# Performance work log

Hardware: AMD Instinct MI355X
Metric: run time of the kernel (lower is better)

The kernel has to match this reference:

```python
import jax, jax.numpy as jnp
import numpy as np

C = 8; E = 512; HEADS = 8; DH = E // HEADS; M = 256; PINV_ITERS = 6; KW = 33

def layer_norm(x, g, b):
    mu = x.mean(-1, keepdims=True)
    xm = x - mu
    v = (xm * xm).mean(-1, keepdims=True)
    return xm / jnp.sqrt(v + 1e-5) * g + b

def mp_pinv(x, iters=PINV_ITERS):
    # Moore-Penrose pseudoinverse via Newton-Schulz iterations (lucidrains nystrom-attention)
    I = jnp.eye(x.shape[-1], dtype=x.dtype)
    ax = jnp.abs(x)
    z = jnp.swapaxes(x, -1, -2) / (jnp.max(ax.sum(-2)) * jnp.max(ax.sum(-1)))
    for _ in range(iters):
        xz = x @ z
        z = 0.25 * z @ (13. * I - xz @ (15. * I - xz @ (7. * I - xz)))
    return z

def nystrom_attn(x, mask, Wqkv, Wout, bout, conv_w):
    b, n0, d = x.shape
    pad = (-n0) % M  # left-pad so seq divisible by num_landmarks
    x = jnp.pad(x, ((0, 0), (pad, 0), (0, 0)))
    mask = jnp.pad(mask, ((0, 0), (pad, 0)))
    n = n0 + pad
    qkv = (x @ Wqkv).reshape(b, n, 3, HEADS, DH).transpose(2, 0, 3, 1, 4)
    q, k, v = qkv[0], qkv[1], qkv[2]  # [b,h,n,dh]
    mf = mask[:, None, :, None].astype(x.dtype)
    q = q * mf * (DH ** -0.5); k = k * mf; v = v * mf
    l = n // M
    mls = mask.reshape(b, 1, M, l).sum(-1).astype(x.dtype)  # valid count per landmark segment
    div = mls[..., None] + 1e-8
    ql = q.reshape(b, HEADS, M, l, DH).sum(3) / div
    kl = k.reshape(b, HEADS, M, l, DH).sum(3) / div
    mland = mls > 0  # [b,1,M]
    neg = -jnp.finfo(x.dtype).max / 2
    sim1 = jnp.where(mask[:, None, :, None] & mland[..., None, :], jnp.einsum('bhid,bhjd->bhij', q, kl), neg)
    sim2 = jnp.where(mland[..., :, None] & mland[..., None, :], jnp.einsum('bhid,bhjd->bhij', ql, kl), neg)
    sim3 = jnp.where(mland[..., :, None] & mask[:, None, None, :], jnp.einsum('bhid,bhjd->bhij', ql, k), neg)
    a1 = jax.nn.softmax(sim1, -1); a2 = jax.nn.softmax(sim2, -1); a3 = jax.nn.softmax(sim3, -1)
    out = (a1 @ mp_pinv(a2)) @ (a3 @ v)
    # residual depthwise conv over sequence dim (residual=True in NystromAttention)
    out = out + jax.lax.conv_general_dilated(v, conv_w, (1, 1), ((KW // 2, KW // 2), (0, 0)),
                                             dimension_numbers=('NCHW', 'OIHW', 'NCHW'),
                                             feature_group_count=HEADS)
    out = out.transpose(0, 2, 1, 3).reshape(b, n, d) @ Wout + bout
    return out[:, pad:]

def _forward(h, W1, b1, cls_token, pmt_token, ln1_g, ln1_b, Wqkv1, Wout1, bout1, conv1,
             ln0_g, ln0_b, Wqkv0, Wout0, bout0, conv0, lnf_g, lnf_b, W3, b3):
    N = h.shape[0]
    h1 = jax.nn.relu(h @ W1 + b1)  # _fc1
    seq = jnp.concatenate([cls_token, pmt_token, h1], 0)[None]  # [1, 1+C+N, E]
    y = nystrom_attn(layer_norm(seq, ln1_g, ln1_b), jnp.ones((1, seq.shape[1]), bool),
                     Wqkv1, Wout1, bout1, conv1)
    x = seq + y  # layer1 (TransLayer_custom)
    pmt = x[:, 1:1 + C, :]   # new pmt tokens [1,C,E]
    toks = x[:, 1 + C:, :]   # [1,N,E]
    assn = jax.nn.softmax(jnp.einsum('bnd,bcd->bnc', toks, pmt), -1)
    idx = jnp.argmax(assn[0], -1)  # [N] cluster assignment
    # cluster dispatch: per-cluster [pmt_i; tokens-of-cluster-i] run of shared layer0, via masking
    xs = jnp.concatenate([pmt[0][:, None, :], jnp.broadcast_to(toks[0], (C, N, E))], 1)  # [C,1+N,E]
    masks = jnp.concatenate([jnp.ones((C, 1), bool), idx[None, :] == jnp.arange(C)[:, None]], 1)
    def trans0(xi, mi):
        xi = xi[None]
        return (xi + nystrom_attn(layer_norm(xi, ln0_g, ln0_b), mi[None], Wqkv0, Wout0, bout0, conv0))[0]
    out = jax.vmap(trans0)(xs, masks)  # [C,1+N,E]
    h_un = out[:, 1:, :][idx, jnp.arange(N)]  # each token from its own cluster's run
    order = jnp.argsort(idx)  # stable: groups tokens by cluster, preserving order (concat order)
    h_global = h_un[order]; idx_new = idx[order]
    hcat = jnp.concatenate([x[0, 0][None], h_global], 0)  # [1+N, E]
    hn = layer_norm(hcat, lnf_g, lnf_b)
    sums = jax.ops.segment_sum(hcat[1:], idx_new, num_segments=C)
    counts = jax.ops.segment_sum(jnp.ones((N,), h.dtype), idx_new, num_segments=C)
    merge = sums / jnp.maximum(counts, 1.)[:, None]  # CTM merge token per cluster
    ptc = jnp.linalg.norm(pmt[0] @ pmt[0].T - jnp.eye(C, dtype=h.dtype))
    tok_out = jnp.concatenate([hn[0][None], merge], 0).mean(0)
    logit = tok_out @ W3 + b3
    return logit, ptc

def setup_inputs() -> dict:
    key = jax.random.key(0)
    ks = jax.random.split(key, 16)
    N, IN_DIM, NC = 4096, 1024, 2
    s = 0.02
    q, _ = jnp.linalg.qr(jax.random.normal(ks[15], (E, C)))  # orthonormal pmt init
    return {
        'h': jax.random.normal(ks[0], (N, IN_DIM)),
        'W1': jax.random.normal(ks[1], (IN_DIM, E)) * s, 'b1': jnp.zeros((E,)),
        'cls_token': jax.random.normal(ks[2], (1, E)),
        'pmt_token': q.T,
        'ln1_g': jnp.ones((E,)), 'ln1_b': jnp.zeros((E,)),
        'Wqkv1': jax.random.normal(ks[3], (E, 3 * E)) * s,
        'Wout1': jax.random.normal(ks[4], (E, E)) * s, 'bout1': jnp.zeros((E,)),
        'conv1': jax.random.normal(ks[5], (HEADS, 1, KW, 1)) * s,
        'ln0_g': jnp.ones((E,)), 'ln0_b': jnp.zeros((E,)),
        'Wqkv0': jax.random.normal(ks[6], (E, 3 * E)) * s,
        'Wout0': jax.random.normal(ks[7], (E, E)) * s, 'bout0': jnp.zeros((E,)),
        'conv0': jax.random.normal(ks[8], (HEADS, 1, KW, 1)) * s,
        'lnf_g': jnp.ones((E,)), 'lnf_b': jnp.zeros((E,)),
        'W3': jax.random.normal(ks[9], (E, NC)) * s, 'b3': jnp.zeros((NC,)),
    }

def reference(h, W1, b1, cls_token, pmt_token, ln1_g, ln1_b, Wqkv1, Wout1, bout1, conv1,
              ln0_g, ln0_b, Wqkv0, Wout0, bout0, conv0, lnf_g, lnf_b, W3, b3):
    logit, ptc = _forward(h, W1, b1, cls_token, pmt_token, ln1_g, ln1_b, Wqkv1, Wout1, bout1, conv1,
                          ln0_g, ln0_b, Wqkv0, Wout0, bout0, conv0, lnf_g, lnf_b, W3, b3)
    return (logit[None], jax.nn.softmax(logit)[None], ptc)
```

## Files before the change

### kernel.cpp

```cpp
#include <hip/hip_runtime.h>

#define NEGV (-1.70141173e38f)

constexpr int E    = 512;
constexpr int NTOK = 4096;
constexpr int NPAD = 4352;
constexpr int PAD1 = 247;
constexpr int NSEQ = 4105;
constexpr int NG   = 5120;

typedef __attribute__((ext_vector_type(8))) short short8;
typedef __attribute__((ext_vector_type(4))) float float4v;

__device__ inline float bf2f(ushort u){ return __uint_as_float(((unsigned)u)<<16); }
__device__ inline ushort f2bf(float f){
  unsigned u = __float_as_uint(f);
  unsigned r = (u + 0x7FFFu + ((u>>16)&1u)) >> 16;
  return (ushort)r;
}

template<int BT, bool BOUNDS>
__global__ __launch_bounds__(256) void k_mm(
    const ushort* __restrict__ A, const ushort* __restrict__ B,
    const float* __restrict__ bias, const float* __restrict__ resid,
    float* __restrict__ Cf, ushort* __restrict__ Cb,
    int M, int N, int K, int ksplit, int ldC,
    long sA, long sB, long sC,
    const int* __restrict__ colsel, const int* __restrict__ rowsel,
    int zmodA, int zmodB, const int* __restrict__ krange, int kshift,
    float alpha, float bdiag, int flags)
{
  const int z = blockIdx.z;
  const int batch = z / ksplit, ks = z - batch * ksplit;
  const int kslice = K / ksplit;
  int kbeg = ks * kslice, kend = kbeg + kslice;
  if (krange) { int ki = batch >> kshift; kbeg = krange[2*ki]; kend = krange[2*ki+1]; }
  long aoff;
  if (colsel) { int s = colsel[blockIdx.x]; if (s < 0) s = 0; aoff = (long)(s*8 + batch) * sA; }
  else aoff = (long)(zmodA ? (batch & (zmodA-1)) : batch) * sA;
  long boff;
  if (rowsel) { int s = rowsel[blockIdx.y]; if (s < 0) s = 0; boff = (long)(s*8 + batch) * sB; }
  else boff = (long)(zmodB ? (batch & (zmodB-1)) : batch) * sB;
  A += aoff; B += boff;
  const long coff = (long)z * sC;

  __shared__ __align__(16) ushort Al[4][128][8];
  __shared__ __align__(16) ushort Bl[4][128][8];

  const int tid  = threadIdx.x;
  const int lane = tid & 63, wid = tid >> 6;
  const int wr = wid >> 1, wc = wid & 1;
  const int l4 = lane >> 4, l15 = lane & 15;
  const int row0 = blockIdx.y * 128, col0 = blockIdx.x * 128;

  float4v acc[4][4];
#pragma unroll
  for (int i = 0; i < 4; ++i)
#pragma unroll
    for (int j = 0; j < 4; ++j) acc[i][j] = (float4v){0.f,0.f,0.f,0.f};

  for (int k0 = kbeg; k0 < kend; k0 += 32) {
    __syncthreads();
#pragma unroll
    for (int e = 0; e < 2; ++e) {
      int id = tid * 2 + e; int m = id >> 2, kb = id & 3;
      uint4 v = make_uint4(0u,0u,0u,0u);
      int gr = row0 + m;
      if (!BOUNDS || gr < M)
        v = *reinterpret_cast<const uint4*>(A + (long)gr * K + k0 + kb * 8);
      *reinterpret_cast<uint4*>(&Al[kb][m][0]) = v;
    }
    if (BT) {
#pragma unroll
      for (int e = 0; e < 2; ++e) {
        int id = tid * 2 + e; int n = id >> 2, kb = id & 3;
        uint4 v = make_uint4(0u,0u,0u,0u);
        int gc = col0 + n;
        if (!BOUNDS || gc < N)
          v = *reinterpret_cast<const uint4*>(B + (long)gc * K + k0 + kb * 8);
        *reinterpret_cast<uint4*>(&Bl[kb][n][0]) = v;
      }
    } else {
      int n = tid & 127, gc = col0 + n;
      bool inb = (!BOUNDS || gc < N);
#pragma unroll
      for (int e = 0; e < 2; ++e) {
        int kb = (tid >> 7) * 2 + e;
        ushort u[8];
#pragma unroll
        for (int j = 0; j < 8; ++j) {
          int gk = k0 + kb * 8 + j;
          ushort val = inb ? B[(long)gk * N + gc] : (ushort)0;
          if (flags & 4) {
            float f = bdiag * (gk == gc ? 1.f : 0.f) - bf2f(val);
            val = f2bf(f);
          }
          u[j] = val;
        }
        uint4 w;
        w.x = (unsigned)u[0] | ((unsigned)u[1] << 16);
        w.y = (unsigned)u[2] | ((unsigned)u[3] << 16);
        w.z = (unsigned)u[4] | ((unsigned)u[5] << 16);
        w.w = (unsigned)u[6] | ((unsigned)u[7] << 16);
        *reinterpret_cast<uint4*>(&Bl[kb][n][0]) = w;
      }
    }
    __syncthreads();
    short8 af[4], bg[4];
#pragma unroll
    for (int mi = 0; mi < 4; ++mi)
      af[mi] = *reinterpret_cast<const short8*>(&Al[l4][wr*64 + mi*16 + l15][0]);
#pragma unroll
    for (int ni = 0; ni < 4; ++ni)
      bg[ni] = *reinterpret_cast<const short8*>(&Bl[l4][wc*64 + ni*16 + l15][0]);
#pragma unroll
    for (int mi = 0; mi < 4; ++mi)
#pragma unroll
      for (int ni = 0; ni < 4; ++ni)
        acc[mi][ni] = __builtin_amdgcn_mfma_f32_16x16x32_bf16(af[mi], bg[ni], acc[mi][ni], 0, 0, 0);
  }
#pragma unroll
  for (int mi = 0; mi < 4; ++mi)
#pragma unroll
    for (int ni = 0; ni < 4; ++ni)
#pragma unroll
      for (int r = 0; r < 4; ++r) {
        int row = row0 + wr*64 + mi*16 + l4*4 + r;
        int col = col0 + wc*64 + ni*16 + l15;
        if (BOUNDS && (row >= M || col >= N)) continue;
        float v = alpha * acc[mi][ni][r];
        if (flags & 1) v += bias[col];
        if (flags & 2) v = fmaxf(v, 0.f);
        if (flags & 8) v += resid[(long)row * ldC + col];
        long off = coff + (long)row * ldC + col;
        if (flags & 16) Cb[off] = f2bf(v); else Cf[off] = v;
      }
}

static void mm(hipStream_t st, const void* A, const void* B, const float* bias, const float* resid,
               float* Cf, ushort* Cb, int M, int N, int K, int nb, int ksplit, int ldC,
               long sA, long sB, long sC,
               const int* colsel, const int* rowsel, int zmodA, int zmodB,
               const int* krange, int kshift,
               float alpha, float bdiag, int flags, bool bt, bool bounds)
{
  dim3 g((N + 127) / 128, (M + 127) / 128, nb * ksplit), b(256);
  const ushort* a = (const ushort*)A; const ushort* bb = (const ushort*)B;
  if (bt) {
    if (bounds) k_mm<1, true ><<<g, b, 0, st>>>(a, bb, bias, resid, Cf, Cb, M, N, K, ksplit, ldC, sA, sB, sC, colsel, rowsel, zmodA, zmodB, krange, kshift, alpha, bdiag, flags);
    else        k_mm<1, false><<<g, b, 0, st>>>(a, bb, bias, resid, Cf, Cb, M, N, K, ksplit, ldC, sA, sB, sC, colsel, rowsel, zmodA, zmodB, krange, kshift, alpha, bdiag, flags);
  } else {
    if (bounds) k_mm<0, true ><<<g, b, 0, st>>>(a, bb, bias, resid, Cf, Cb, M, N, K, ksplit, ldC, sA, sB, sC, colsel, rowsel, zmodA, zmodB, krange, kshift, alpha, bdiag, flags);
    else        k_mm<0, false><<<g, b, 0, st>>>(a, bb, bias, resid, Cf, Cb, M, N, K, ksplit, ldC, sA, sB, sC, colsel, rowsel, zmodA, zmodB, krange, kshift, alpha, bdiag, flags);
  }
}

__global__ void k_copy(const float* __restrict__ s, float* __restrict__ d, int n) {
  int i = blockIdx.x * 256 + threadIdx.x;
  if (i < n) d[i] = s[i];
}
__global__ void k_cvt(const float* __restrict__ s, ushort* __restrict__ d, long n) {
  long i = (long)blockIdx.x * 256 + threadIdx.x;
  if (i < n) d[i] = f2bf(s[i]);
}
__global__ void k_tcvt(const float* __restrict__ W, ushort* __restrict__ Wt, int K, int N) {
  __shared__ float tile[32][33];
  int kb = blockIdx.y * 32, nb_ = blockIdx.x * 32;
  int tx = threadIdx.x, ty = threadIdx.y;
  for (int r = ty; r < 32; r += 8) tile[r][tx] = W[(long)(kb + r) * N + nb_ + tx];
  __syncthreads();
  for (int r = ty; r < 32; r += 8) Wt[(long)(nb_ + r) * K + kb + tx] = f2bf(tile[tx][r]);
}

__global__ __launch_bounds__(256) void k_ln(const float* __restrict__ x, const float* __restrict__ g,
                                            const float* __restrict__ b, ushort* __restrict__ y, int rows) {
  int row = blockIdx.x;
  if (row >= rows) return;
  const float* xr = x + (long)row * E;
  __shared__ float red[256];
  int t = threadIdx.x;
  float v0 = xr[t], v1 = xr[t + 256];
  red[t] = v0 + v1; __syncthreads();
  for (int o = 128; o > 0; o >>= 1) { if (t < o) red[t] += red[t + o]; __syncthreads(); }
  float mu = red[0] * (1.f / E); __syncthreads();
  float d0 = v0 - mu, d1 = v1 - mu;
  red[t] = d0 * d0 + d1 * d1; __syncthreads();
  for (int o = 128; o > 0; o >>= 1) { if (t < o) red[t] += red[t + o]; __syncthreads(); }
  float inv = 1.f / sqrtf(red[0] * (1.f / E) + 1e-5f);
  ushort* yr = y + (long)row * E;
  yr[t]       = f2bf(d0 * inv * g[t]       + b[t]);
  yr[t + 256] = f2bf(d1 * inv * g[t + 256] + b[t + 256]);
}

__global__ void k_buildK(const float* __restrict__ qkv, ushort* __restrict__ Kb, int np, int off) {
  long i = (long)blockIdx.x * 256 + threadIdx.x;
  if (i >= (long)np * 512) return;
  int p = (int)(i >> 9), t = (int)(i & 511); int h = t >> 6, d = t & 63;
  Kb[((long)h * np + p) * 64 + d] = f2bf(qkv[(long)p * 1536 + off + t]);
}
__global__ void k_buildVt(const float* __restrict__ qkv, ushort* __restrict__ Vt, int np) {
  int h = blockIdx.y, p0 = blockIdx.x * 64;
  __shared__ float tile[64][65];
  int tx = threadIdx.x & 63, tg = threadIdx.x >> 6;
  for (int r = tg; r < 64; r += 4) tile[r][tx] = qkv[(long)(p0 + r) * 1536 + 1024 + h * 64 + tx];
  __syncthreads();
  for (int d = tg; d < 64; d += 4) Vt[((long)h * 64 + d) * np + p0 + tx] = f2bf(tile[tx][d]);
}

__global__ void k_lm_B(float* __restrict__ divB, float* __restrict__ mlandB) {
  int i = threadIdx.x;
  int cnt = 0;
  for (int j = 0; j < 17; ++j) cnt += (i * 17 + j >= PAD1);
  divB[i] = (float)cnt + 1e-8f;
  mlandB[i] = cnt > 0 ? 1.f : 0.f;
}
__global__ void k_qlkl_B(const float* __restrict__ qkv, const float* __restrict__ divB,
                         ushort* __restrict__ ql, ushort* __restrict__ kl) {
  int i = blockIdx.x, h = blockIdx.y, d = threadIdx.x;
  float sq = 0.f, sk = 0.f;
  for (int j = 0; j < 17; ++j) {
    int p = i * 17 + j;
    if (p >= PAD1) {
      sq += qkv[(long)p * 1536 + h * 64 + d];
      sk += qkv[(long)p * 1536 + 512 + h * 64 + d];
    }
  }
  float dv = divB[i];
  ql[((long)h * 256 + i) * 64 + d] = f2bf(sq * 0.125f / dv);
  kl[((long)h * 256 + i) * 64 + d] = f2bf(sk / dv);
}

__global__ __launch_bounds__(256) void k_a2soft(const float* __restrict__ S2, const float* __restrict__ mland,
                                                ushort* __restrict__ X) {
  int i = blockIdx.x, bt = blockIdx.y, j = threadIdx.x;
  int cl = bt >> 3;
  const float* Sr = S2 + ((long)bt * 256 + i) * 256;
  __shared__ float red[256];
  float landi = mland[cl * 256 + i];
  float out;
  if (landi > 0.f) {
    bool valid = mland[cl * 256 + j] > 0.f;
    float sv = valid ? Sr[j] : NEGV;
    red[j] = sv; __syncthreads();
    for (int o = 128; o > 0; o >>= 1) { if (j < o) red[j] = fmaxf(red[j], red[j + o]); __syncthreads(); }
    float mx = red[0]; __syncthreads();
    float e = valid ? expf(sv - mx) : 0.f;
    red[j] = e; __syncthreads();
    for (int o = 128; o > 0; o >>= 1) { if (j < o) red[j] += red[j + o]; __syncthreads(); }
    out = e / red[0];
  } else {
    out = 1.f / 256.f;
  }
  X[((long)bt * 256 + i) * 256 + j] = f2bf(out);
}

__global__ __launch_bounds__(256) void k_pinv_scale(const ushort* __restrict__ X, float* __restrict__ sc, int nheads) {
  int cl = blockIdx.x, j = threadIdx.x;
  float cmax = -1e30f, rmax = -1e30f;
  for (int h = 0; h < nheads; ++h) {
    const ushort* mat = X + (long)(cl * nheads + h) * 65536;
    float cs = 0.f, rs = 0.f;
    for (int i = 0; i < 256; ++i) { cs += bf2f(mat[i * 256 + j]); rs += bf2f(mat[j * 256 + i]); }
    cmax = fmaxf(cmax, cs); rmax = fmaxf(rmax, rs);
  }
  __shared__ float r1[256], r2[256];
  r1[j] = cmax; r2[j] = rmax; __syncthreads();
  for (int o = 128; o > 0; o >>= 1) {
    if (j < o) { r1[j] = fmaxf(r1[j], r1[j + o]); r2[j] = fmaxf(r2[j], r2[j + o]); }
    __syncthreads();
  }
  if (j == 0) sc[cl] = 1.f / (r1[0] * r2[0]);
}

__global__ void k_z0(const ushort* __restrict__ X, const float* __restrict__ sc, ushort* __restrict__ Z, int nb) {
  long t = (long)blockIdx.x * 256 + threadIdx.x;
  if (t >= (long)nb * 65536) return;
  int bt = (int)(t >> 16); int ij = (int)(t & 65535); int i = ij >> 8, j = ij & 255;
  Z[t] = f2bf(bf2f(X[((long)bt << 16) + j * 256 + i]) * sc[bt >> 3]);
}

__global__ __launch_bounds__(256) void k_smaxB_av(const float* __restrict__ S, ushort* __restrict__ P,
                                                  const float* __restrict__ mland) {
  int i = blockIdx.x, h = blockIdx.y, t = threadIdx.x;
  const float* Sr = S + ((long)h * 256 + i) * NPAD;
  ushort* Pr = P + ((long)h * 256 + i) * NPAD;
  __shared__ float sv[NPAD];
  __shared__ float red[256];
  if (mland[i] > 0.f) {
    float lmax = NEGV;
    for (int j = t; j < NPAD; j += 256) {
      float s = Sr[j];
      sv[j] = s;
      if (j >= PAD1) lmax = fmaxf(lmax, s);
    }
    red[t] = lmax; __syncthreads();
    for (int o = 128; o > 0; o >>= 1) { if (t < o) red[t] = fmaxf(red[t], red[t + o]); __syncthreads(); }
    float mx = red[0]; __syncthreads();
    float lsum = 0.f;
    for (int j = t; j < NPAD; j += 256) {
      float e = (j >= PAD1) ? expf(sv[j] - mx) : 0.f;
      sv[j] = e; lsum += e;
    }
    red[t] = lsum; __syncthreads();
    for (int o = 128; o > 0; o >>= 1) { if (t < o) red[t] += red[t + o]; __syncthreads(); }
    float inv = 1.f / red[0];
    for (int j = t; j < NPAD; j += 256) Pr[j] = f2bf(sv[j] * inv);
  } else {
    const float u = 1.f / 4352.f;
    for (int j = t; j < NPAD; j += 256) Pr[j] = f2bf(j >= PAD1 ? u : 0.f);
  }
}

__global__ __launch_bounds__(256) void k_smaxseg(const float* __restrict__ S3, ushort* __restrict__ P3,
                                                 const float* __restrict__ mlandC, const int* __restrict__ gclu,
                                                 const int* __restrict__ segb) {
  int i = blockIdx.x, bt = blockIdx.y, t = threadIdx.x;
  int c = bt >> 3, h = bt & 7;
  const float* Sr = S3 + ((long)h * 256 + i) * NG;
  ushort* Pr = P3 + ((long)h * 256 + i) * NG;
  int jb = segb[c], je = segb[c + 1];
  __shared__ float sv[4352];
  __shared__ float red[256];
  if (mlandC[c * 256 + i] > 0.f) {
    float lmax = NEGV;
    for (int j = jb + t; j < je; j += 256) {
      float s = Sr[j];
      sv[j - jb] = s;
      if (gclu[j] == c) lmax = fmaxf(lmax, s);
    }
    red[t] = lmax; __syncthreads();
    for (int o = 128; o > 0; o >>= 1) { if (t < o) red[t] = fmaxf(red[t], red[t + o]); __syncthreads(); }
    float mx = red[0]; __syncthreads();
    float lsum = 0.f;
    for (int j = jb + t; j < je; j += 256) {
      float e = (gclu[j] == c) ? expf(sv[j - jb] - mx) : 0.f;
      sv[j - jb] = e; lsum += e;
    }
    red[t] = lsum; __syncthreads();
    for (int o = 128; o > 0; o >>= 1) { if (t < o) red[t] += red[t + o]; __syncthreads(); }
    float inv = 1.f / red[0];
    for (int j = jb + t; j < je; j += 256) Pr[j] = f2bf(sv[j - jb] * inv);
  } else {
    const float u = 1.f / 4352.f;
    for (int j = jb + t; j < je; j += 256) Pr[j] = f2bf(gclu[j] == c ? u : 0.f);
  }
}

template<int MODE>
__global__ __launch_bounds__(256) void k_smax256(const float* __restrict__ S, ushort* __restrict__ P,
                                                 const float* __restrict__ mland, const int* __restrict__ gtok,
                                                 const int* __restrict__ gclu, int rows) {
  int row = blockIdx.x, h = blockIdx.y, j = threadIdx.x;
  const float* Sr = S + ((long)h * rows + row) * 256;
  ushort* Pr = P + ((long)h * rows + row) * 256;
  int c = 0;
  if (MODE == 1) {
    int tk = gtok[row];
    if (tk < 0) { Pr[j] = 0; return; }
    c = gclu[row];
  }
  bool mem = (MODE == 1) ? (mland[c * 256 + j] > 0.f) : (mland[j] > 0.f);
  __shared__ float red[256];
  float s = mem ? Sr[j] : NEGV;
  red[j] = s; __syncthreads();
  for (int o = 128; o > 0; o >>= 1) { if (j < o) red[j] = fmaxf(red[j], red[j + o]); __syncthreads(); }
  float mx = red[0]; __syncthreads();
  float e = mem ? expf(s - mx) : 0.f;
  red[j] = e; __syncthreads();
  for (int o = 128; o > 0; o >>= 1) { if (j < o) red[j] += red[j + o]; __syncthreads(); }
  Pr[j] = f2bf(e / red[0]);
}

__global__ void k_avredB(const float* __restrict__ sl, ushort* __restrict__ avb, int ks) {
  int i = blockIdx.x, h = blockIdx.y, d = threadIdx.x;
  float s = 0.f;
  for (int k = 0; k < ks; ++k) s += sl[(((long)h * ks + k) * 256 + i) * 64 + d];
  avb[((long)h * 256 + i) * 64 + d] = f2bf(s);
}

__global__ void k_conv_B(const float* __restrict__ qkv, const float* __restrict__ w, float* __restrict__ preout) {
  int prow = PAD1 + blockIdx.x, t = threadIdx.x;
  int h = t >> 6;
  float acc = 0.f;
  for (int tt = 0; tt < 33; ++tt) {
    int p = prow + tt - 16;
    if (p >= 0 && p < NPAD) acc += qkv[(long)p * 1536 + 1024 + t] * w[h * 33 + tt];
  }
  preout[(long)prow * E + t] += acc;
}

__global__ void k_idx(const float* __restrict__ x, int* __restrict__ idx) {
  int n = blockIdx.x;
  const float* tok = x + (long)(9 + n) * E;
  const float* pmt = x + E;
  __shared__ float red[64];
  int t = threadIdx.x;
  int c = t >> 3, part = t & 7;
  float s = 0.f;
  for (int d = part * 64; d < part * 64 + 64; ++d) s += tok[d] * pmt[(long)c * E + d];
  red[t] = s; __syncthreads();
  if (t < 8) {
    float dot = 0.f;
    for (int p = 0; p < 8; ++p) dot += red[t * 8 + p];
    red[t] = dot;
  }
  __syncthreads();
  if (t == 0) {
    int best = 0; float bv = red[0];
    for (int c2 = 1; c2 < 8; ++c2) if (red[c2] > bv) { bv = red[c2]; best = c2; }
    idx[n] = best;
  }
}

__global__ void k_ptc(const float* __restrict__ x, float* __restrict__ ptc_out) {
  int t = threadIdx.x;
  int a = t >> 3, b = t & 7;
  const float* pmt = x + E;
  float s = 0.f;
  for (int d = 0; d < E; ++d) s += pmt[(long)a * E + d] * pmt[(long)b * E + d];
  s -= (a == b) ? 1.f : 0.f;
  __shared__ float red[64];
  red[t] = s * s; __syncthreads();
  for (int o = 32; o > 0; o >>= 1) { if (t < o) red[t] += red[t + o]; __syncthreads(); }
  if (t == 0) *ptc_out = sqrtf(red[0]);
}

__global__ void k_lm_C(const int* __restrict__ idx, float* __restrict__ div_c, float* __restrict__ mland_c) {
  int c = blockIdx.x, i = threadIdx.x;
  int cnt = 0;
  for (int j = 0; j < 17; ++j) {
    int p = i * 17 + j;
    if (p == 255) cnt++;
    else if (p >= 256 && idx[p - 256] == c) cnt++;
  }
  div_c[c * 256 + i] = (float)cnt + 1e-8f;
  mland_c[c * 256 + i] = cnt > 0 ? 1.f : 0.f;
}

__global__ void k_qlkl_C(const float* __restrict__ qkv, const float* __restrict__ qkv_pmt,
                         const int* __restrict__ idx, const float* __restrict__ div_c,
                         ushort* __restrict__ qlc, ushort* __restrict__ klc) {
  int i = blockIdx.x, bt = blockIdx.y;
  int c = bt >> 3, h = bt & 7, d = threadIdx.x;
  float sq = 0.f, sk = 0.f;
  for (int j = 0; j < 17; ++j) {
    int p = i * 17 + j;
    const float* src = nullptr;
    if (p == 255) src = qkv_pmt + c * 1536;
    else if (p >= 256 && idx[p - 256] == c) src = qkv + (long)(p - 256) * 1536;
    if (src) { sq += src[h * 64 + d]; sk += src[512 + h * 64 + d]; }
  }
  float dv = div_c[c * 256 + i];
  qlc[((long)bt * 256 + i) * 64 + d] = f2bf(sq * 0.125f / dv);
  klc[((long)bt * 256 + i) * 64 + d] = f2bf(sk / dv);
}

__global__ void k_gcnt(const int* __restrict__ idx, int* __restrict__ scnt) {
  __shared__ int loc[8];
  int b = blockIdx.x, t = threadIdx.x;
  if (t < 8) loc[t] = 0;
  __syncthreads();
  atomicAdd(&loc[idx[b * 256 + t]], 1);
  __syncthreads();
  if (t < 8) scnt[t * 16 + b] = loc[t];
}

__global__ void k_goff(const int* __restrict__ scnt, int* __restrict__ segb, int* __restrict__ boff,
                       int* __restrict__ krange, int* __restrict__ blkclu,
                       int* __restrict__ gtok, int* __restrict__ gclu) {
  if (threadIdx.x != 0) return;
  int s = 0;
  for (int c = 0; c < 8; ++c) {
    segb[c] = s;
    int tot = 1;
    int run = s + 1;
    for (int sl = 0; sl < 16; ++sl) { boff[c * 16 + sl] = run; run += scnt[c * 16 + sl]; tot += scnt[c * 16 + sl]; }
    krange[2 * c] = s;
    krange[2 * c + 1] = s + (((tot + 31) >> 5) << 5);
    gtok[s] = -2 - c; gclu[s] = c;
    s += ((tot + 127) >> 7) << 7;
  }
  segb[8] = s;
  for (int b = 0; b < NG / 128; ++b) {
    int cl = -1;
    for (int c = 0; c < 8; ++c) if (b * 128 >= segb[c] && b * 128 < segb[c + 1]) cl = c;
    blkclu[b] = cl;
  }
}

__global__ void k_gscatter(const int* __restrict__ idx, const int* __restrict__ boff,
                           int* __restrict__ gtok, int* __restrict__ gclu, int* __restrict__ gpos) {
  __shared__ int sidx[256];
  int b = blockIdx.x, t = threadIdx.x;
  int n = b * 256 + t;
  int c = idx[n];
  sidx[t] = c;
  __syncthreads();
  int rank = 0;
  for (int m = 0; m < t; ++m) rank += (sidx[m] == c);
  int pos = boff[c * 16 + b] + rank;
  gtok[pos] = n; gclu[pos] = c; gpos[n] = pos;
}

__global__ void k_gatherQK(const float* __restrict__ qkv, const float* __restrict__ qkv_pmt,
                           const int* __restrict__ gtok, ushort* __restrict__ Qg, ushort* __restrict__ Kg) {
  long i = (long)blockIdx.x * 256 + threadIdx.x;
  if (i >= (long)NG * 512) return;
  int g = (int)(i >> 9), t = (int)(i & 511); int h = t >> 6, d = t & 63;
  int tk = gtok[g];
  float q = 0.f, k = 0.f;
  if (tk >= 0)       { q = qkv[(long)tk * 1536 + t];      k = qkv[(long)tk * 1536 + 512 + t]; }
  else if (tk <= -2) { int c = -2 - tk; q = qkv_pmt[c * 1536 + t]; k = qkv_pmt[c * 1536 + 512 + t]; }
  long o = ((long)h * NG + g) * 64 + d;
  Qg[o] = f2bf(q); Kg[o] = f2bf(k);
}

__global__ void k_gatherVt(const float* __restrict__ qkv, const float* __restrict__ qkv_pmt,
                           const int* __restrict__ gtok, ushort* __restrict__ Vgt) {
  int h = blockIdx.y, p0 = blockIdx.x * 64;
  __shared__ float tile[64][65];
  int tx = threadIdx.x & 63, tg = threadIdx.x >> 6;
  for (int r = tg; r < 64; r += 4) {
    int tk = gtok[p0 + r];
    float v = 0.f;
    if (tk >= 0)       v = qkv[(long)tk * 1536 + 1024 + h * 64 + tx];
    else if (tk <= -2) v = qkv_pmt[(-2 - tk) * 1536 + 1024 + h * 64 + tx];
    tile[r][tx] = v;
  }
  __syncthreads();
  for (int d = tg; d < 64; d += 4) Vgt[((long)h * 64 + d) * NG + p0 + tx] = f2bf(tile[tx][d]);
}

__global__ void k_outC(const float* __restrict__ OUTg, const int* __restrict__ gpos,
                       const int* __restrict__ idx, const float* __restrict__ qkv,
                       const float* __restrict__ qkv_pmt, const float* __restrict__ w,
                       float* __restrict__ OUTA) {
  int n = blockIdx.x, t = threadIdx.x;
  int h = t >> 6;
  int c = idx[n];
  float acc = OUTg[(long)gpos[n] * 512 + t];
  for (int tt = 0; tt < 33; ++tt) {
    int m = n + tt - 16;
    float vv = 0.f;
    if (m == -1) vv = qkv_pmt[c * 1536 + 1024 + t];
    else if (m >= 0 && m < NTOK && idx[m] == c) vv = qkv[(long)m * 1536 + 1024 + t];
    acc += vv * w[h * 33 + tt];
  }
  OUTA[(long)n * E + t] = acc;
}

__global__ void k_seg_part(const float* __restrict__ hun, const int* __restrict__ idx,
                           float* __restrict__ part, float* __restrict__ pcnt) {
  int c = blockIdx.x, sl = blockIdx.y, d = threadIdx.x;
  float s = 0.f; int cnt = 0;
  for (int n = sl * 256; n < sl * 256 + 256; ++n) {
    if (idx[n] == c) { s += hun[(long)n * E + d]; if (d == 0) cnt++; }
  }
  part[(long)(c * 16 + sl) * E + d] = s;
  if (d == 0) pcnt[c * 16 + sl] = (float)cnt;
}

__global__ void k_final(const float* __restrict__ x0, const float* __restrict__ g, const float* __restrict__ b,
                        const float* __restrict__ part, const float* __restrict__ pcnt,
                        const float* __restrict__ ptc, const float* __restrict__ W3, const float* __restrict__ b3,
                        float* __restrict__ out) {
  int t = threadIdx.x;
  __shared__ float red[512];
  float xv = x0[t];
  red[t] = xv; __syncthreads();
  for (int o = 256; o > 0; o >>= 1) { if (t < o) red[t] += red[t + o]; __syncthreads(); }
  float mu = red[0] * (1.f / 512.f); __syncthreads();
  float d0 = xv - mu;
  red[t] = d0 * d0; __syncthreads();
  for (int o = 256; o > 0; o >>= 1) { if (t < o) red[t] += red[t + o]; __syncthreads(); }
  float inv = 1.f / sqrtf(red[0] * (1.f / 512.f) + 1e-5f);
  __syncthreads();
  float acc = d0 * inv * g[t] + b[t];
  for (int c = 0; c < 8; ++c) {
    float s = 0.f, cnt = 0.f;
    for (int sl = 0; sl < 16; ++sl) { s += part[(long)(c * 16 + sl) * E + t]; cnt += pcnt[c * 16 + sl]; }
    acc += s / fmaxf(cnt, 1.f);
  }
  float tk = acc * (1.f / 9.f);
  red[t] = tk * W3[t * 2 + 0]; __syncthreads();
  for (int o = 256; o > 0; o >>= 1) { if (t < o) red[t] += red[t + o]; __syncthreads(); }
  float l0 = red[0] + b3[0]; __syncthreads();
  red[t] = tk * W3[t * 2 + 1]; __syncthreads();
  for (int o = 256; o > 0; o >>= 1) { if (t < o) red[t] += red[t + o]; __syncthreads(); }
  float l1 = red[0] + b3[1];
  if (t == 0) {
    out[0] = l0; out[1] = l1;
    float mx = fmaxf(l0, l1);
    float e0 = expf(l0 - mx), e1 = expf(l1 - mx), s = e0 + e1;
    out[2] = e0 / s; out[3] = e1 / s;
    out[4] = *ptc;
  }
}

static void pinv_iters(hipStream_t st, const ushort* PX, ushort* PZ, ushort* Y, ushort* T1, ushort* T2, int nb) {
  ushort* z = PZ; ushort* y = Y;
  for (int it = 0; it < 6; ++it) {
    mm(st, PX, z,  nullptr, nullptr, nullptr, y,  256,256,256, nb,1,256, 65536,65536,65536, nullptr,nullptr,0,0,nullptr,0, 1.f,   0.f, 16,    false, false);
    mm(st, y,  y,  nullptr, nullptr, nullptr, T1, 256,256,256, nb,1,256, 65536,65536,65536, nullptr,nullptr,0,0,nullptr,0, 1.f,   7.f, 16|4,  false, false);
    mm(st, y,  T1, nullptr, nullptr, nullptr, T2, 256,256,256, nb,1,256, 65536,65536,65536, nullptr,nullptr,0,0,nullptr,0, 1.f,  15.f, 16|4,  false, false);
    mm(st, z,  T2, nullptr, nullptr, nullptr, y,  256,256,256, nb,1,256, 65536,65536,65536, nullptr,nullptr,0,0,nullptr,0, 0.25f,13.f, 16|4,  false, false);
    ushort* tmp = z; z = y; y = tmp;
  }
}

extern "C" void kernel_launch(void* const* d_in, const int* in_sizes, int n_in,
                              void* d_out, int out_size, void* d_ws, size_t ws_size,
                              hipStream_t stream) {
  const float* h_in  = (const float*)d_in[0];
  const float* W1    = (const float*)d_in[1];
  const float* b1    = (const float*)d_in[2];
  const float* cls   = (const float*)d_in[3];
  const float* pmt_t = (const float*)d_in[4];
  const float* ln1_g = (const float*)d_in[5];
  const float* ln1_b = (const float*)d_in[6];
  const float* Wqkv1 = (const float*)d_in[7];
  const float* Wout1 = (const float*)d_in[8];
  const float* bout1 = (const float*)d_in[9];
  const float* conv1 = (const float*)d_in[10];
  const float* ln0_g = (const float*)d_in[11];
  const float* ln0_b = (const float*)d_in[12];
  const float* Wqkv0 = (const float*)d_in[13];
  const float* Wout0 = (const float*)d_in[14];
  const float* bout0 = (const float*)d_in[15];
  const float* conv0 = (const float*)d_in[16];
  const float* lnf_g = (const float*)d_in[17];
  const float* lnf_b = (const float*)d_in[18];
  const float* W3    = (const float*)d_in[19];
  const float* b3    = (const float*)d_in[20];

  char* base = (char*)d_ws;
  size_t off = 0;
  auto alloc = [&](size_t b) -> void* {
    off = (off + 255) & ~(size_t)255;
    void* p = base + off; off += b; return p;
  };
  float*  SEQ    = (float*) alloc((size_t)NSEQ * E * 4);
  float*  QKV    = (float*) alloc((size_t)NPAD * 1536 * 4);
  float*  QKVPMT = (float*) alloc(8 * 1536 * 4);
  ushort* W1t    = (ushort*)alloc((size_t)512 * 1024 * 2);
  ushort* Wq1t   = (ushort*)alloc((size_t)1536 * 512 * 2);
  ushort* Wq0t   = (ushort*)alloc((size_t)1536 * 512 * 2);
  ushort* Wo1t   = (ushort*)alloc((size_t)512 * 512 * 2);
  ushort* Wo0t   = (ushort*)alloc((size_t)512 * 512 * 2);
  ushort* LNb    = (ushort*)alloc((size_t)NPAD * E * 2);
  ushort* LNPMTb = (ushort*)alloc(8 * 512 * 2);
  ushort* QbU    = (ushort*)alloc((size_t)8 * NG * 64 * 2);
  ushort* KbU    = (ushort*)alloc((size_t)8 * NG * 64 * 2);
  ushort* VtU    = (ushort*)alloc((size_t)8 * NG * 64 * 2);
  char*   U1     = (char*)  alloc((size_t)8 * 256 * NG * 4);
  char*   U2     = (char*)  alloc((size_t)8 * 256 * NG * 2);
  ushort* PXb    = (ushort*)alloc((size_t)64 * 65536 * 2);
  ushort* PZa    = (ushort*)alloc((size_t)64 * 65536 * 2);
  ushort* qlbB   = (ushort*)alloc((size_t)8 * 16384 * 2);
  ushort* klbB   = (ushort*)alloc((size_t)8 * 16384 * 2);
  ushort* qlcb   = (ushort*)alloc((size_t)64 * 16384 * 2);
  ushort* klcb   = (ushort*)alloc((size_t)64 * 16384 * 2);
  float*  avsl   = (float*) alloc((size_t)8 * 8 * 16384 * 4);
  ushort* avb    = (ushort*)alloc((size_t)64 * 16384 * 2);
  ushort* Wcb    = (ushort*)alloc((size_t)64 * 16384 * 2);
  float*  PREOUT = (float*) alloc((size_t)NPAD * E * 4);
  float*  OUTA   = (float*) alloc((size_t)NTOK * E * 4);
  float*  divB   = (float*) alloc(256 * 4);
  float*  mlandB = (float*) alloc(256 * 4);
  float*  divC   = (float*) alloc(8 * 256 * 4);
  float*  mlandC = (float*) alloc(8 * 256 * 4);
  int*    idx    = (int*)   alloc(NTOK * 4);
  int*    gtok   = (int*)   alloc(NG * 4);
  int*    gclu   = (int*)   alloc(NG * 4);
  int*    gpos   = (int*)   alloc(NTOK * 4);
  int*    scnt   = (int*)   alloc(8 * 16 * 4);
  int*    boffA  = (int*)   alloc(8 * 16 * 4);
  int*    segb   = (int*)   alloc(9 * 4);
  int*    krange = (int*)   alloc(16 * 4);
  int*    blkclu = (int*)   alloc((NG / 128) * 4);
  float*  ptc    = (float*) alloc(256);
  float*  sc     = (float*) alloc(256);
  float*  part   = (float*) alloc((size_t)8 * 16 * 512 * 4);
  float*  pcnt   = (float*) alloc(8 * 16 * 4);

  ushort* hb   = (ushort*)U1;
  float*  Sbuf = (float*)U1;
  ushort* Ybuf = (ushort*)U1;
  ushort* T1   = (ushort*)(U1 + (size_t)64 * 65536 * 2);
  ushort* T2   = (ushort*)(U1 + (size_t)2 * 64 * 65536 * 2);
  float*  OUTg = (float*)U1;
  ushort* Pbuf = (ushort*)U2;

  k_tcvt<<<dim3(512/32, 1024/32), dim3(32,8), 0, stream>>>(W1, W1t, 1024, 512);
  k_tcvt<<<dim3(1536/32, 512/32), dim3(32,8), 0, stream>>>(Wqkv1, Wq1t, 512, 1536);
  k_tcvt<<<dim3(1536/32, 512/32), dim3(32,8), 0, stream>>>(Wqkv0, Wq0t, 512, 1536);
  k_tcvt<<<dim3(512/32, 512/32),  dim3(32,8), 0, stream>>>(Wout1, Wo1t, 512, 512);
  k_tcvt<<<dim3(512/32, 512/32),  dim3(32,8), 0, stream>>>(Wout0, Wo0t, 512, 512);

  k_copy<<<dim3(2),  dim3(256), 0, stream>>>(cls,   SEQ,       512);
  k_copy<<<dim3(16), dim3(256), 0, stream>>>(pmt_t, SEQ + 512, 4096);
  k_cvt<<<dim3(16384), dim3(256), 0, stream>>>(h_in, hb, (long)4096 * 1024);
  mm(stream, hb, W1t, b1, nullptr, SEQ + 9 * 512, nullptr, 4096, 512, 1024, 1, 1, 512,
     0, 0, 0, nullptr, nullptr, 0, 0, nullptr, 0, 1.f, 0.f, 1 | 2, true, false);

  hipMemsetAsync(LNb, 0, (size_t)PAD1 * E * 2, stream);
  k_ln<<<dim3(NSEQ), dim3(256), 0, stream>>>(SEQ, ln1_g, ln1_b, LNb + (long)PAD1 * E, NSEQ);
  mm(stream, LNb, Wq1t, nullptr, nullptr, QKV, nullptr, NPAD, 1536, 512, 1, 1, 1536,
     0, 0, 0, nullptr, nullptr, 0, 0, nullptr, 0, 1.f, 0.f, 0, true, false);
  k_buildK<<<dim3((NPAD*512)/256), dim3(256), 0, stream>>>(QKV, QbU, NPAD, 0);
  k_buildK<<<dim3((NPAD*512)/256), dim3(256), 0, stream>>>(QKV, KbU, NPAD, 512);
  k_buildVt<<<dim3(NPAD/64, 8), dim3(256), 0, stream>>>(QKV, VtU, NPAD);
  k_lm_B<<<dim3(1), dim3(256), 0, stream>>>(divB, mlandB);
  k_qlkl_B<<<dim3(256, 8), dim3(64), 0, stream>>>(QKV, divB, qlbB, klbB);
  mm(stream, qlbB, klbB, nullptr, nullptr, Sbuf, nullptr, 256, 256, 64, 8, 1, 256,
     16384, 16384, 65536, nullptr, nullptr, 0, 0, nullptr, 0, 1.f, 0.f, 0, true, false);
  k_a2soft<<<dim3(256, 8), dim3(256), 0, stream>>>(Sbuf, mlandB, PXb);
  k_pinv_scale<<<dim3(1), dim3(256), 0, stream>>>(PXb, sc, 8);
  k_z0<<<dim3((8*65536)/256), dim3(256), 0, stream>>>(PXb, sc, PZa, 8);
  pinv_iters(stream, PXb, PZa, Ybuf, T1, T2, 8);
  mm(stream, qlbB, KbU, nullptr, nullptr, Sbuf, nullptr, 256, NPAD, 64, 8, 1, NPAD,
     16384, (long)NPAD*64, (long)256*NPAD, nullptr, nullptr, 0, 0, nullptr, 0, 1.f, 0.f, 0, true, false);
  k_smaxB_av<<<dim3(256, 8), dim3(256), 0, stream>>>(Sbuf, Pbuf, mlandB);
  mm(stream, Pbuf, VtU, nullptr, nullptr, avsl, nullptr, 256, 64, NPAD, 8, 8, 64,
     (long)256*NPAD, (long)64*NPAD, 16384, nullptr, nullptr, 0, 0, nullptr, 0, 1.f, 0.f, 0, true, true);
  k_avredB<<<dim3(256, 8), dim3(64), 0, stream>>>(avsl, avb, 8);
  mm(stream, PZa, avb, nullptr, nullptr, nullptr, Wcb, 256, 64, 256, 8, 1, 64,
     65536, 16384, 16384, nullptr, nullptr, 0, 0, nullptr, 0, 1.f, 0.f, 16, false, true);
  mm(stream, QbU + PAD1*64, klbB, nullptr, nullptr, Sbuf, nullptr, NSEQ, 256, 64, 8, 1, 256,
     (long)NPAD*64, 16384, (long)NSEQ*256, nullptr, nullptr, 0, 0, nullptr, 0, 0.125f, 0.f, 0, true, true);
  k_smax256<0><<<dim3(NSEQ, 8), dim3(256), 0, stream>>>(Sbuf, Pbuf, mlandB, nullptr, nullptr, NSEQ);
  mm(stream, Pbuf, Wcb, nullptr, nullptr, PREOUT + (long)PAD1*512, nullptr, NSEQ, 64, 256, 8, 1, 512,
     (long)NSEQ*256, 16384, 64, nullptr, nullptr, 0, 0, nullptr, 0, 1.f, 0.f, 0, false, true);
  k_conv_B<<<dim3(NSEQ), dim3(512), 0, stream>>>(QKV, conv1, PREOUT);
  k_cvt<<<dim3((NSEQ*512 + 255)/256), dim3(256), 0, stream>>>(PREOUT + (long)PAD1*E, LNb, (long)NSEQ * 512);
  mm(stream, LNb, Wo1t, bout1, SEQ, SEQ, nullptr, NSEQ, 512, 512, 1, 1, 512,
     0, 0, 0, nullptr, nullptr, 0, 0, nullptr, 0, 1.f, 0.f, 1 | 8, true, true);

  k_idx<<<dim3(NTOK), dim3(64), 0, stream>>>(SEQ, idx);
  k_ptc<<<dim3(1), dim3(64), 0, stream>>>(SEQ, ptc);
  hipMemsetAsync(gtok, 0xFF, NG * 4, stream);
  hipMemsetAsync(gclu, 0xFF, NG * 4, stream);
  k_gcnt<<<dim3(16), dim3(256), 0, stream>>>(idx, scnt);
  k_goff<<<dim3(1), dim3(64), 0, stream>>>(scnt, segb, boffA, krange, blkclu, gtok, gclu);
  k_gscatter<<<dim3(16), dim3(256), 0, stream>>>(idx, boffA, gtok, gclu, gpos);
  k_ln<<<dim3(NTOK), dim3(256), 0, stream>>>(SEQ + 9 * 512, ln0_g, ln0_b, LNb, NTOK);
  k_ln<<<dim3(8), dim3(256), 0, stream>>>(SEQ + 512, ln0_g, ln0_b, LNPMTb, 8);
  mm(stream, LNb, Wq0t, nullptr, nullptr, QKV, nullptr, NTOK, 1536, 512, 1, 1, 1536,
     0, 0, 0, nullptr, nullptr, 0, 0, nullptr, 0, 1.f, 0.f, 0, true, false);
  mm(stream, LNPMTb, Wq0t, nullptr, nullptr, QKVPMT, nullptr, 8, 1536, 512, 1, 1, 1536,
     0, 0, 0, nullptr, nullptr, 0, 0, nullptr, 0, 1.f, 0.f, 0, true, true);
  k_lm_C<<<dim3(8), dim3(256), 0, stream>>>(idx, divC, mlandC);
  k_qlkl_C<<<dim3(256, 64), dim3(64), 0, stream>>>(QKV, QKVPMT, idx, divC, qlcb, klcb);
  k_gatherQK<<<dim3((NG*512)/256), dim3(256), 0, stream>>>(QKV, QKVPMT, gtok, QbU, KbU);
  k_gatherVt<<<dim3(NG/64, 8), dim3(256), 0, stream>>>(QKV, QKVPMT, gtok, VtU);
  mm(stream, qlcb, klcb, nullptr, nullptr, Sbuf, nullptr, 256, 256, 64, 64, 1, 256,
     16384, 16384, 65536, nullptr, nullptr, 0, 0, nullptr, 0, 1.f, 0.f, 0, true, false);
  k_a2soft<<<dim3(256, 64), dim3(256), 0, stream>>>(Sbuf, mlandC, PXb);
  k_pinv_scale<<<dim3(8), dim3(256), 0, stream>>>(PXb, sc, 8);
  k_z0<<<dim3((64*65536)/256), dim3(256), 0, stream>>>(PXb, sc, PZa, 64);
  pinv_iters(stream, PXb, PZa, Ybuf, T1, T2, 64);
  mm(stream, qlcb, KbU, nullptr, nullptr, Sbuf, nullptr, 256, NG, 64, 8, 1, NG,
     16384, (long)NG*64, (long)256*NG, blkclu, nullptr, 0, 0, nullptr, 0, 1.f, 0.f, 0, true, false);
  k_smaxseg<<<dim3(256, 64), dim3(256), 0, stream>>>(Sbuf, Pbuf, mlandC, gclu, segb);
  mm(stream, Pbuf, VtU, nullptr, nullptr, nullptr, avb, 256, 64, NG, 64, 1, 64,
     (long)256*NG, (long)64*NG, 16384, nullptr, nullptr, 8, 8, krange, 3, 1.f, 0.f, 16, true, true);
  mm(stream, PZa, avb, nullptr, nullptr, nullptr, Wcb, 256, 64, 256, 64, 1, 64,
     65536, 16384, 16384, nullptr, nullptr, 0, 0, nullptr, 0, 1.f, 0.f, 16, false, true);
  mm(stream, QbU, klcb, nullptr, nullptr, Sbuf, nullptr, NG, 256, 64, 8, 1, 256,
     (long)NG*64, 16384, (long)NG*256, nullptr, blkclu, 0, 0, nullptr, 0, 0.125f, 0.f, 0, true, false);
  k_smax256<1><<<dim3(NG, 8), dim3(256), 0, stream>>>(Sbuf, Pbuf, mlandC, gtok, gclu, NG);
  mm(stream, Pbuf, Wcb, nullptr, nullptr, OUTg, nullptr, NG, 64, 256, 8, 1, 512,
     (long)NG*256, 16384, 64, nullptr, blkclu, 0, 0, nullptr, 0, 1.f, 0.f, 0, false, true);
  k_outC<<<dim3(NTOK), dim3(512), 0, stream>>>(OUTg, gpos, idx, QKV, QKVPMT, conv0, OUTA);
  k_cvt<<<dim3((NTOK*512)/256), dim3(256), 0, stream>>>(OUTA, LNb, (long)NTOK * 512);
  mm(stream, LNb, Wo0t, bout0, SEQ + 9 * 512, PREOUT, nullptr, NTOK, 512, 512, 1, 1, 512,
     0, 0, 0, nullptr, nullptr, 0, 0, nullptr, 0, 1.f, 0.f, 1 | 8, true, false);

  k_seg_part<<<dim3(8, 16), dim3(512), 0, stream>>>(PREOUT, idx, part, pcnt);
  k_final<<<dim3(1), dim3(512), 0, stream>>>(SEQ, lnf_g, lnf_b, part, pcnt, ptc, W3, b3,
                                             (float*)d_out);
}
```

Baseline: 2.712 ms.

## Fuse pinv Newton-Schulz loop into one kernel and merge many small kernels

```diff
diff --git a/kernel.cpp b/kernel.cpp
--- a/kernel.cpp
+++ b/kernel.cpp
@@ -8,6 +8,7 @@
 constexpr int PAD1 = 247;
 constexpr int NSEQ = 4105;
 constexpr int NG   = 5120;
+constexpr int NTP  = 4104;
 
 typedef __attribute__((ext_vector_type(8))) short short8;
 typedef __attribute__((ext_vector_type(4))) float float4v;
@@ -17,6 +18,14 @@
   unsigned u = __float_as_uint(f);
   unsigned r = (u + 0x7FFFu + ((u>>16)&1u)) >> 16;
   return (ushort)r;
+}
+__device__ inline short8 pack8u(const ushort* u) {
+  union { short8 v; unsigned w[4]; } x;
+  x.w[0] = (unsigned)u[0] | ((unsigned)u[1] << 16);
+  x.w[1] = (unsigned)u[2] | ((unsigned)u[3] << 16);
+  x.w[2] = (unsigned)u[4] | ((unsigned)u[5] << 16);
+  x.w[3] = (unsigned)u[6] | ((unsigned)u[7] << 16);
+  return x.v;
 }
 
 template<int BT, bool BOUNDS>
@@ -155,30 +164,227 @@
   }
 }
 
-__global__ void k_copy(const float* __restrict__ s, float* __restrict__ d, int n) {
+__device__ __forceinline__ void gsync() {
+  __threadfence();
+  __syncthreads();
+}
+
+template<int AMODE, int BMODE>
+__device__ __forceinline__ void wg_gemm256(
+    const ushort* __restrict__ Ag, const ushort* __restrict__ Bg,
+    ushort (* __restrict__ Yl)[256], ushort (* __restrict__ Btl)[256],
+    float4v acc[8][4], int tid)
+{
+  const int lane = tid & 63;
+  const int wid  = tid >> 6;
+  const int wr = wid >> 2, wc = wid & 3;
+  const int l4 = lane >> 4, l15 = lane & 15;
+#pragma unroll 1
+  for (int kt = 0; kt < 8; ++kt) {
+    const int k0 = kt * 32;
+    if (BMODE == 0) {
+      __syncthreads();
+      int kk = tid >> 4, n0 = (tid & 15) * 16;
+      int s = (kk >> 3) << 4;
+      const ushort* src = Bg + (long)(k0 + kk) * 256 + n0;
+      *reinterpret_cast<uint4*>(&Btl[kk][n0 ^ s])       = *reinterpret_cast<const uint4*>(src);
+      *reinterpret_cast<uint4*>(&Btl[kk][(n0 + 8) ^ s]) = *reinterpret_cast<const uint4*>(src + 8);
+      __syncthreads();
+    }
+    short8 af[8];
+#pragma unroll
+    for (int mi = 0; mi < 8; ++mi) {
+      int r = wr * 128 + mi * 16 + l15;
+      if (AMODE == 0) {
+        af[mi] = *reinterpret_cast<const short8*>(Ag + (long)r * 256 + k0 + l4 * 8);
+      } else {
+        int sr = ((r >> 3) & 3) << 4;
+        af[mi] = *reinterpret_cast<const short8*>(&Yl[r][(k0 + l4 * 8) ^ sr]);
+      }
+    }
+    short8 bf[4];
+#pragma unroll
+    for (int ni = 0; ni < 4; ++ni) {
+      int c = wc * 64 + ni * 16 + l15;
+      ushort u[8];
+      if (BMODE == 0) {
+        int kb = l4 * 8;
+        int cc = c ^ ((kb >> 3) << 4);
+#pragma unroll
+        for (int j = 0; j < 8; ++j) u[j] = Btl[kb + j][cc];
+      } else {
+        int kb = k0 + l4 * 8;
+        int cc = c ^ (((kb >> 3) & 3) << 4);
+#pragma unroll
+        for (int j = 0; j < 8; ++j) u[j] = Yl[kb + j][cc];
+      }
+      bf[ni] = pack8u(u);
+    }
+#pragma unroll
+    for (int mi = 0; mi < 8; ++mi)
+#pragma unroll
+      for (int ni = 0; ni < 4; ++ni)
+        acc[mi][ni] = __builtin_amdgcn_mfma_f32_16x16x32_bf16(af[mi], bf[ni], acc[mi][ni], 0, 0, 0);
+  }
+}
+
+__global__ __launch_bounds__(512) void k_pinv_chain(
+    const ushort* __restrict__ Xall, ushort* __restrict__ ZAall, ushort* __restrict__ ZBall,
+    ushort* __restrict__ T1all, ushort* __restrict__ T2all, const float* __restrict__ sc)
+{
+  __shared__ ushort Yl[256][256];
+  __shared__ ushort Btl[32][256];
+  const int bt = blockIdx.x;
+  const ushort* X = Xall + (long)bt * 65536;
+  ushort* Z0 = ZAall + (long)bt * 65536;
+  ushort* Z1 = ZBall + (long)bt * 65536;
+  ushort* T1 = T1all + (long)bt * 65536;
+  ushort* T2 = T2all + (long)bt * 65536;
+  const int tid = threadIdx.x;
+  const int lane = tid & 63, wid = tid >> 6;
+  const int wr = wid >> 2, wc = wid & 3;
+  const int l4 = lane >> 4, l15 = lane & 15;
+  const float scale = sc[bt >> 3];
+
+  {
+    int r = tid & 255, half = tid >> 8;
+    for (int c0 = half * 128; c0 < half * 128 + 128; c0 += 8) {
+      ushort u[8];
+#pragma unroll
+      for (int j = 0; j < 8; ++j)
+        u[j] = f2bf(bf2f(X[(long)(c0 + j) * 256 + r]) * scale);
+      *reinterpret_cast<short8*>(Z0 + (long)r * 256 + c0) = pack8u(u);
+    }
+  }
+  gsync();
+
+  ushort* Zc = Z0;
+  ushort* Zn = Z1;
+  float4v acc[8][4];
+
+  for (int it = 0; it < 6; ++it) {
+#pragma unroll
+    for (int i = 0; i < 8; ++i)
+#pragma unroll
+      for (int j = 0; j < 4; ++j) acc[i][j] = (float4v){0.f,0.f,0.f,0.f};
+    wg_gemm256<0,0>(X, Zc, Yl, Btl, acc, tid);
+    __syncthreads();
+#pragma unroll
+    for (int mi = 0; mi < 8; ++mi)
+#pragma unroll
+      for (int ni = 0; ni < 4; ++ni)
+#pragma unroll
+        for (int ri = 0; ri < 4; ++ri) {
+          int row = wr*128 + mi*16 + l4*4 + ri;
+          int col = wc*64 + ni*16 + l15;
+          Yl[row][col ^ (((row >> 3) & 3) << 4)] = f2bf(acc[mi][ni][ri]);
+        }
+    __syncthreads();
+#pragma unroll
+    for (int i = 0; i < 8; ++i)
+#pragma unroll
+      for (int j = 0; j < 4; ++j) acc[i][j] = (float4v){0.f,0.f,0.f,0.f};
+    wg_gemm256<1,1>(nullptr, nullptr, Yl, Btl, acc, tid);
+#pragma unroll
+    for (int mi = 0; mi < 8; ++mi)
+#pragma unroll
+      for (int ni = 0; ni < 4; ++ni)
+#pragma unroll
+        for (int ri = 0; ri < 4; ++ri) {
+          int row = wr*128 + mi*16 + l4*4 + ri;
+          int col = wc*64 + ni*16 + l15;
+          float y = bf2f(Yl[row][col ^ (((row >> 3) & 3) << 4)]);
+          T1[(long)row*256 + col] = f2bf(7.f*y - acc[mi][ni][ri]);
+        }
+    gsync();
+#pragma unroll
+    for (int i = 0; i < 8; ++i)
+#pragma unroll
+      for (int j = 0; j < 4; ++j) acc[i][j] = (float4v){0.f,0.f,0.f,0.f};
+    wg_gemm256<1,0>(nullptr, T1, Yl, Btl, acc, tid);
+#pragma unroll
+    for (int mi = 0; mi < 8; ++mi)
+#pragma unroll
+      for (int ni = 0; ni < 4; ++ni)
+#pragma unroll
+        for (int ri = 0; ri < 4; ++ri) {
+          int row = wr*128 + mi*16 + l4*4 + ri;
+          int col = wc*64 + ni*16 + l15;
+          float y = bf2f(Yl[row][col ^ (((row >> 3) & 3) << 4)]);
+          T2[(long)row*256 + col] = f2bf(15.f*y - acc[mi][ni][ri]);
+        }
+    gsync();
+#pragma unroll
+    for (int i = 0; i < 8; ++i)
+#pragma unroll
+      for (int j = 0; j < 4; ++j) acc[i][j] = (float4v){0.f,0.f,0.f,0.f};
+    wg_gemm256<0,0>(Zc, T2, Yl, Btl, acc, tid);
+#pragma unroll
+    for (int mi = 0; mi < 8; ++mi)
+#pragma unroll
+      for (int ni = 0; ni < 4; ++ni)
+#pragma unroll
+        for (int ri = 0; ri < 4; ++ri) {
+          int row = wr*128 + mi*16 + l4*4 + ri;
+          int col = wc*64 + ni*16 + l15;
+          float zv = bf2f(Zc[(long)row*256 + col]);
+          Zn[(long)row*256 + col] = f2bf(0.25f*(13.f*zv - acc[mi][ni][ri]));
+        }
+    gsync();
+    ushort* tmp = Zc; Zc = Zn; Zn = tmp;
+  }
+}
+
+__global__ __launch_bounds__(256) void k_colmax(const ushort* __restrict__ X, float* __restrict__ sc) {
+  int cl = blockIdx.x, j = threadIdx.x;
+  float cmax = 0.f;
+  for (int h = 0; h < 8; ++h) {
+    const ushort* mat = X + (long)(cl * 8 + h) * 65536;
+    float cs = 0.f;
+    for (int i = 0; i < 256; ++i) cs += bf2f(mat[i * 256 + j]);
+    cmax = fmaxf(cmax, cs);
+  }
+  __shared__ float red[256];
+  red[j] = cmax; __syncthreads();
+  for (int o = 128; o > 0; o >>= 1) { if (j < o) red[j] = fmaxf(red[j], red[j + o]); __syncthreads(); }
+  if (j == 0) sc[cl] = 1.f / red[0];
+}
+
+__global__ void k_prep0(const float* __restrict__ cls, const float* __restrict__ pmt, float* __restrict__ seq) {
   int i = blockIdx.x * 256 + threadIdx.x;
-  if (i < n) d[i] = s[i];
+  if (i < 512) seq[i] = cls[i];
+  else if (i < 4608) seq[i] = pmt[i - 512];
 }
 __global__ void k_cvt(const float* __restrict__ s, ushort* __restrict__ d, long n) {
   long i = (long)blockIdx.x * 256 + threadIdx.x;
   if (i < n) d[i] = f2bf(s[i]);
 }
-__global__ void k_tcvt(const float* __restrict__ W, ushort* __restrict__ Wt, int K, int N) {
+__global__ void k_tcvt_all(const float* __restrict__ W1, const float* __restrict__ Wq1,
+                           const float* __restrict__ Wq0, const float* __restrict__ Wo1,
+                           const float* __restrict__ Wo0,
+                           ushort* __restrict__ W1t, ushort* __restrict__ Wq1t,
+                           ushort* __restrict__ Wq0t, ushort* __restrict__ Wo1t,
+                           ushort* __restrict__ Wo0t) {
+  const float* W; ushort* Wt; int K, N;
+  switch (blockIdx.z) {
+    case 0:  W = W1;  Wt = W1t;  K = 1024; N = 512;  break;
+    case 1:  W = Wq1; Wt = Wq1t; K = 512;  N = 1536; break;
+    case 2:  W = Wq0; Wt = Wq0t; K = 512;  N = 1536; break;
+    case 3:  W = Wo1; Wt = Wo1t; K = 512;  N = 512;  break;
+    default: W = Wo0; Wt = Wo0t; K = 512;  N = 512;  break;
+  }
+  int nb_ = blockIdx.x * 32, kb = blockIdx.y * 32;
+  if (nb_ >= N || kb >= K) return;
   __shared__ float tile[32][33];
-  int kb = blockIdx.y * 32, nb_ = blockIdx.x * 32;
   int tx = threadIdx.x, ty = threadIdx.y;
   for (int r = ty; r < 32; r += 8) tile[r][tx] = W[(long)(kb + r) * N + nb_ + tx];
   __syncthreads();
   for (int r = ty; r < 32; r += 8) Wt[(long)(nb_ + r) * K + kb + tx] = f2bf(tile[tx][r]);
 }
 
-__global__ __launch_bounds__(256) void k_ln(const float* __restrict__ x, const float* __restrict__ g,
-                                            const float* __restrict__ b, ushort* __restrict__ y, int rows) {
-  int row = blockIdx.x;
-  if (row >= rows) return;
-  const float* xr = x + (long)row * E;
-  __shared__ float red[256];
-  int t = threadIdx.x;
+__device__ __forceinline__ void ln_row(const float* __restrict__ xr, const float* __restrict__ g,
+                                       const float* __restrict__ b, ushort* __restrict__ yr,
+                                       float* red, int t) {
   float v0 = xr[t], v1 = xr[t + 256];
   red[t] = v0 + v1; __syncthreads();
   for (int o = 128; o > 0; o >>= 1) { if (t < o) red[t] += red[t + o]; __syncthreads(); }
@@ -187,47 +393,101 @@
   red[t] = d0 * d0 + d1 * d1; __syncthreads();
   for (int o = 128; o > 0; o >>= 1) { if (t < o) red[t] += red[t + o]; __syncthreads(); }
   float inv = 1.f / sqrtf(red[0] * (1.f / E) + 1e-5f);
-  ushort* yr = y + (long)row * E;
   yr[t]       = f2bf(d0 * inv * g[t]       + b[t]);
   yr[t + 256] = f2bf(d1 * inv * g[t + 256] + b[t + 256]);
 }
 
-__global__ void k_buildK(const float* __restrict__ qkv, ushort* __restrict__ Kb, int np, int off) {
-  long i = (long)blockIdx.x * 256 + threadIdx.x;
-  if (i >= (long)np * 512) return;
-  int p = (int)(i >> 9), t = (int)(i & 511); int h = t >> 6, d = t & 63;
-  Kb[((long)h * np + p) * 64 + d] = f2bf(qkv[(long)p * 1536 + off + t]);
-}
-__global__ void k_buildVt(const float* __restrict__ qkv, ushort* __restrict__ Vt, int np) {
+__global__ __launch_bounds__(256) void k_lnB(const float* __restrict__ x, const float* __restrict__ g,
+                                             const float* __restrict__ b, ushort* __restrict__ y) {
+  int row = blockIdx.x, t = threadIdx.x;
+  ushort* yr = y + (long)row * E;
+  if (row < PAD1) { yr[t] = 0; yr[t + 256] = 0; return; }
+  __shared__ float red[256];
+  ln_row(x + (long)(row - PAD1) * E, g, b, yr, red, t);
+}
+__global__ __launch_bounds__(256) void k_lnC(const float* __restrict__ seq, const float* __restrict__ g,
+                                             const float* __restrict__ b, ushort* __restrict__ y) {
+  int row = blockIdx.x, t = threadIdx.x;
+  const float* xr = (row < 8) ? (seq + 512 + (long)row * E) : (seq + 9 * 512 + (long)(row - 8) * E);
+  __shared__ float red[256];
+  ln_row(xr, g, b, y + (long)row * E, red, t);
+}
+
+__global__ void k_buildQKVB(const float* __restrict__ qkv, ushort* __restrict__ Qb,
+                            ushort* __restrict__ Kb, ushort* __restrict__ Vt) {
   int h = blockIdx.y, p0 = blockIdx.x * 64;
+  int tx = threadIdx.x & 63, tg = threadIdx.x >> 6;
   __shared__ float tile[64][65];
+  for (int r = tg; r < 64; r += 4) {
+    long src = (long)(p0 + r) * 1536 + h * 64 + tx;
+    long o = ((long)h * NPAD + p0 + r) * 64 + tx;
+    Qb[o] = f2bf(qkv[src]);
+    Kb[o] = f2bf(qkv[src + 512]);
+    tile[r][tx] = qkv[src + 1024];
+  }
+  __syncthreads();
+  for (int d = tg; d < 64; d += 4) Vt[((long)h * 64 + d) * NPAD + p0 + tx] = f2bf(tile[tx][d]);
+}
+__global__ void k_gatherQKV(const float* __restrict__ qkvall, const int* __restrict__ gtok,
+                            ushort* __restrict__ Qg, ushort* __restrict__ Kg, ushort* __restrict__ Vgt) {
+  int h = blockIdx.y, p0 = blockIdx.x * 64;
   int tx = threadIdx.x & 63, tg = threadIdx.x >> 6;
-  for (int r = tg; r < 64; r += 4) tile[r][tx] = qkv[(long)(p0 + r) * 1536 + 1024 + h * 64 + tx];
+  __shared__ float tile[64][65];
+  for (int r = tg; r < 64; r += 4) {
+    int tk = gtok[p0 + r];
+    int srcrow = tk >= 0 ? 8 + tk : (tk <= -2 ? (-2 - tk) : -1);
+    float q = 0.f, k = 0.f, v = 0.f;
+    if (srcrow >= 0) {
+      long s = (long)srcrow * 1536 + h * 64 + tx;
+      q = qkvall[s]; k = qkvall[s + 512]; v = qkvall[s + 1024];
+    }
+    long o = ((long)h * NG + p0 + r) * 64 + tx;
+    Qg[o] = f2bf(q); Kg[o] = f2bf(k);
+    tile[r][tx] = v;
+  }
   __syncthreads();
-  for (int d = tg; d < 64; d += 4) Vt[((long)h * 64 + d) * np + p0 + tx] = f2bf(tile[tx][d]);
-}
-
-__global__ void k_lm_B(float* __restrict__ divB, float* __restrict__ mlandB) {
-  int i = threadIdx.x;
-  int cnt = 0;
-  for (int j = 0; j < 17; ++j) cnt += (i * 17 + j >= PAD1);
-  divB[i] = (float)cnt + 1e-8f;
-  mlandB[i] = cnt > 0 ? 1.f : 0.f;
-}
-__global__ void k_qlkl_B(const float* __restrict__ qkv, const float* __restrict__ divB,
-                         ushort* __restrict__ ql, ushort* __restrict__ kl) {
+  for (int d = tg; d < 64; d += 4) Vgt[((long)h * 64 + d) * NG + p0 + tx] = f2bf(tile[tx][d]);
+}
+
+__global__ void k_qlkl_B(const float* __restrict__ qkv, ushort* __restrict__ ql, ushort* __restrict__ kl,
+                         float* __restrict__ mlandB) {
   int i = blockIdx.x, h = blockIdx.y, d = threadIdx.x;
-  float sq = 0.f, sk = 0.f;
+  float sq = 0.f, sk = 0.f; int cnt = 0;
   for (int j = 0; j < 17; ++j) {
     int p = i * 17 + j;
     if (p >= PAD1) {
       sq += qkv[(long)p * 1536 + h * 64 + d];
       sk += qkv[(long)p * 1536 + 512 + h * 64 + d];
-    }
-  }
-  float dv = divB[i];
+      cnt++;
+    }
+  }
+  float dv = (float)cnt + 1e-8f;
   ql[((long)h * 256 + i) * 64 + d] = f2bf(sq * 0.125f / dv);
   kl[((long)h * 256 + i) * 64 + d] = f2bf(sk / dv);
+  if (h == 0 && d == 0) mlandB[i] = cnt > 0 ? 1.f : 0.f;
+}
+
+__global__ void k_qlkl_C(const float* __restrict__ qkvall, const int* __restrict__ idx,
+                         ushort* __restrict__ qlc, ushort* __restrict__ klc,
+                         float* __restrict__ mland_c) {
+  int i = blockIdx.x, bt = blockIdx.y;
+  int c = bt >> 3, h = bt & 7, d = threadIdx.x;
+  float sq = 0.f, sk = 0.f; int cnt = 0;
+  for (int j = 0; j < 17; ++j) {
+    int p = i * 17 + j;
+    int srcrow = -1;
+    if (p == 255) srcrow = c;
+    else if (p >= 256 && idx[p - 256] == c) srcrow = 8 + (p - 256);
+    if (srcrow >= 0) {
+      const float* src = qkvall + (long)srcrow * 1536 + h * 64;
+      sq += src[d]; sk += src[512 + d];
+      cnt++;
+    }
+  }
+  float dv = (float)cnt + 1e-8f;
+  qlc[((long)bt * 256 + i) * 64 + d] = f2bf(sq * 0.125f / dv);
+  klc[((long)bt * 256 + i) * 64 + d] = f2bf(sk / dv);
+  if (h == 0 && d == 0) mland_c[c * 256 + i] = cnt > 0 ? 1.f : 0.f;
 }
 
 __global__ __launch_bounds__(256) void k_a2soft(const float* __restrict__ S2, const float* __restrict__ mland,
@@ -254,31 +514,6 @@
   X[((long)bt * 256 + i) * 256 + j] = f2bf(out);
 }
 
-__global__ __launch_bounds__(256) void k_pinv_scale(const ushort* __restrict__ X, float* __restrict__ sc, int nheads) {
-  int cl = blockIdx.x, j = threadIdx.x;
-  float cmax = -1e30f, rmax = -1e30f;
-  for (int h = 0; h < nheads; ++h) {
-    const ushort* mat = X + (long)(cl * nheads + h) * 65536;
-    float cs = 0.f, rs = 0.f;
-    for (int i = 0; i < 256; ++i) { cs += bf2f(mat[i * 256 + j]); rs += bf2f(mat[j * 256 + i]); }
-    cmax = fmaxf(cmax, cs); rmax = fmaxf(rmax, rs);
-  }
-  __shared__ float r1[256], r2[256];
-  r1[j] = cmax; r2[j] = rmax; __syncthreads();
-  for (int o = 128; o > 0; o >>= 1) {
-    if (j < o) { r1[j] = fmaxf(r1[j], r1[j + o]); r2[j] = fmaxf(r2[j], r2[j + o]); }
-    __syncthreads();
-  }
-  if (j == 0) sc[cl] = 1.f / (r1[0] * r2[0]);
-}
-
-__global__ void k_z0(const ushort* __restrict__ X, const float* __restrict__ sc, ushort* __restrict__ Z, int nb) {
-  long t = (long)blockIdx.x * 256 + threadIdx.x;
-  if (t >= (long)nb * 65536) return;
-  int bt = (int)(t >> 16); int ij = (int)(t & 65535); int i = ij >> 8, j = ij & 255;
-  Z[t] = f2bf(bf2f(X[((long)bt << 16) + j * 256 + i]) * sc[bt >> 3]);
-}
-
 __global__ __launch_bounds__(256) void k_smaxB_av(const float* __restrict__ S, ushort* __restrict__ P,
                                                   const float* __restrict__ mland) {
   int i = blockIdx.x, h = blockIdx.y, t = threadIdx.x;
@@ -378,23 +613,36 @@
   avb[((long)h * 256 + i) * 64 + d] = f2bf(s);
 }
 
-__global__ void k_conv_B(const float* __restrict__ qkv, const float* __restrict__ w, float* __restrict__ preout) {
-  int prow = PAD1 + blockIdx.x, t = threadIdx.x;
+__global__ void k_conv_B(const float* __restrict__ qkv, const float* __restrict__ w,
+                         const float* __restrict__ preout, ushort* __restrict__ lnb) {
+  int r = blockIdx.x, t = threadIdx.x;
   int h = t >> 6;
-  float acc = 0.f;
+  int prow = PAD1 + r;
+  float acc = preout[(long)prow * E + t];
   for (int tt = 0; tt < 33; ++tt) {
     int p = prow + tt - 16;
-    if (p >= 0 && p < NPAD) acc += qkv[(long)p * 1536 + 1024 + t] * w[h * 33 + tt];
-  }
-  preout[(long)prow * E + t] += acc;
-}
-
-__global__ void k_idx(const float* __restrict__ x, int* __restrict__ idx) {
+    if (p < NPAD) acc += qkv[(long)p * 1536 + 1024 + t] * w[h * 33 + tt];
+  }
+  lnb[(long)r * E + t] = f2bf(acc);
+}
+
+__global__ void k_idxptc(const float* __restrict__ x, int* __restrict__ idx, float* __restrict__ ptc_out) {
+  int t = threadIdx.x;
+  __shared__ float red[64];
+  if (blockIdx.x == NTOK) {
+    int a = t >> 3, b = t & 7;
+    const float* pmt = x + E;
+    float s = 0.f;
+    for (int d = 0; d < E; ++d) s += pmt[(long)a * E + d] * pmt[(long)b * E + d];
+    s -= (a == b) ? 1.f : 0.f;
+    red[t] = s * s; __syncthreads();
+    for (int o = 32; o > 0; o >>= 1) { if (t < o) red[t] += red[t + o]; __syncthreads(); }
+    if (t == 0) *ptc_out = sqrtf(red[0]);
+    return;
+  }
   int n = blockIdx.x;
   const float* tok = x + (long)(9 + n) * E;
   const float* pmt = x + E;
-  __shared__ float red[64];
-  int t = threadIdx.x;
   int c = t >> 3, part = t & 7;
   float s = 0.f;
   for (int d = part * 64; d < part * 64 + 64; ++d) s += tok[d] * pmt[(long)c * E + d];
@@ -412,129 +660,57 @@
   }
 }
 
-__global__ void k_ptc(const float* __restrict__ x, float* __restrict__ ptc_out) {
+__global__ __launch_bounds__(256) void k_gprep(const int* __restrict__ idx, int* __restrict__ gtok,
+                                               int* __restrict__ gclu, int* __restrict__ gpos,
+                                               int* __restrict__ segb, int* __restrict__ krange,
+                                               int* __restrict__ blkclu) {
+  __shared__ int hist[8][16];
+  __shared__ int boff[8][16];
+  __shared__ int segs[9];
+  __shared__ int sidx[256];
   int t = threadIdx.x;
-  int a = t >> 3, b = t & 7;
-  const float* pmt = x + E;
-  float s = 0.f;
-  for (int d = 0; d < E; ++d) s += pmt[(long)a * E + d] * pmt[(long)b * E + d];
-  s -= (a == b) ? 1.f : 0.f;
-  __shared__ float red[64];
-  red[t] = s * s; __syncthreads();
-  for (int o = 32; o > 0; o >>= 1) { if (t < o) red[t] += red[t + o]; __syncthreads(); }
-  if (t == 0) *ptc_out = sqrtf(red[0]);
-}
-
-__global__ void k_lm_C(const int* __restrict__ idx, float* __restrict__ div_c, float* __restrict__ mland_c) {
-  int c = blockIdx.x, i = threadIdx.x;
-  int cnt = 0;
-  for (int j = 0; j < 17; ++j) {
-    int p = i * 17 + j;
-    if (p == 255) cnt++;
-    else if (p >= 256 && idx[p - 256] == c) cnt++;
-  }
-  div_c[c * 256 + i] = (float)cnt + 1e-8f;
-  mland_c[c * 256 + i] = cnt > 0 ? 1.f : 0.f;
-}
-
-__global__ void k_qlkl_C(const float* __restrict__ qkv, const float* __restrict__ qkv_pmt,
-                         const int* __restrict__ idx, const float* __restrict__ div_c,
-                         ushort* __restrict__ qlc, ushort* __restrict__ klc) {
-  int i = blockIdx.x, bt = blockIdx.y;
-  int c = bt >> 3, h = bt & 7, d = threadIdx.x;
-  float sq = 0.f, sk = 0.f;
-  for (int j = 0; j < 17; ++j) {
-    int p = i * 17 + j;
-    const float* src = nullptr;
-    if (p == 255) src = qkv_pmt + c * 1536;
-    else if (p >= 256 && idx[p - 256] == c) src = qkv + (long)(p - 256) * 1536;
-    if (src) { sq += src[h * 64 + d]; sk += src[512 + h * 64 + d]; }
-  }
-  float dv = div_c[c * 256 + i];
-  qlc[((long)bt * 256 + i) * 64 + d] = f2bf(sq * 0.125f / dv);
-  klc[((long)bt * 256 + i) * 64 + d] = f2bf(sk / dv);
-}
-
-__global__ void k_gcnt(const int* __restrict__ idx, int* __restrict__ scnt) {
-  __shared__ int loc[8];
-  int b = blockIdx.x, t = threadIdx.x;
-  if (t < 8) loc[t] = 0;
+  if (t < 128) ((int*)hist)[t] = 0;
   __syncthreads();
-  atomicAdd(&loc[idx[b * 256 + t]], 1);
+  for (int b = 0; b < 16; ++b) atomicAdd(&hist[idx[b * 256 + t]][b], 1);
   __syncthreads();
-  if (t < 8) scnt[t * 16 + b] = loc[t];
-}
-
-__global__ void k_goff(const int* __restrict__ scnt, int* __restrict__ segb, int* __restrict__ boff,
-                       int* __restrict__ krange, int* __restrict__ blkclu,
-                       int* __restrict__ gtok, int* __restrict__ gclu) {
-  if (threadIdx.x != 0) return;
-  int s = 0;
-  for (int c = 0; c < 8; ++c) {
-    segb[c] = s;
-    int tot = 1;
-    int run = s + 1;
-    for (int sl = 0; sl < 16; ++sl) { boff[c * 16 + sl] = run; run += scnt[c * 16 + sl]; tot += scnt[c * 16 + sl]; }
-    krange[2 * c] = s;
-    krange[2 * c + 1] = s + (((tot + 31) >> 5) << 5);
-    gtok[s] = -2 - c; gclu[s] = c;
-    s += ((tot + 127) >> 7) << 7;
-  }
-  segb[8] = s;
-  for (int b = 0; b < NG / 128; ++b) {
+  if (t == 0) {
+    int s = 0;
+    for (int c = 0; c < 8; ++c) {
+      segs[c] = s;
+      int run = s + 1, tot = 1;
+      for (int b = 0; b < 16; ++b) { boff[c][b] = run; run += hist[c][b]; tot += hist[c][b]; }
+      krange[2 * c] = s;
+      krange[2 * c + 1] = s + ((tot + 31) & ~31);
+      s += (tot + 127) & ~127;
+    }
+    segs[8] = s;
+    for (int c = 0; c <= 8; ++c) segb[c] = segs[c];
+  }
+  __syncthreads();
+  for (int g = t; g < NG; g += 256) { gtok[g] = -1; gclu[g] = -1; }
+  __syncthreads();
+  if (t < 8) { gtok[segs[t]] = -2 - t; gclu[segs[t]] = t; }
+  for (int b = t; b < NG / 128; b += 256) {
     int cl = -1;
-    for (int c = 0; c < 8; ++c) if (b * 128 >= segb[c] && b * 128 < segb[c + 1]) cl = c;
+    for (int c = 0; c < 8; ++c) if (b * 128 >= segs[c] && b * 128 < segs[c + 1]) cl = c;
     blkclu[b] = cl;
   }
-}
-
-__global__ void k_gscatter(const int* __restrict__ idx, const int* __restrict__ boff,
-                           int* __restrict__ gtok, int* __restrict__ gclu, int* __restrict__ gpos) {
-  __shared__ int sidx[256];
-  int b = blockIdx.x, t = threadIdx.x;
-  int n = b * 256 + t;
-  int c = idx[n];
-  sidx[t] = c;
-  __syncthreads();
-  int rank = 0;
-  for (int m = 0; m < t; ++m) rank += (sidx[m] == c);
-  int pos = boff[c * 16 + b] + rank;
-  gtok[pos] = n; gclu[pos] = c; gpos[n] = pos;
-}
-
-__global__ void k_gatherQK(const float* __restrict__ qkv, const float* __restrict__ qkv_pmt,
-                           const int* __restrict__ gtok, ushort* __restrict__ Qg, ushort* __restrict__ Kg) {
-  long i = (long)blockIdx.x * 256 + threadIdx.x;
-  if (i >= (long)NG * 512) return;
-  int g = (int)(i >> 9), t = (int)(i & 511); int h = t >> 6, d = t & 63;
-  int tk = gtok[g];
-  float q = 0.f, k = 0.f;
-  if (tk >= 0)       { q = qkv[(long)tk * 1536 + t];      k = qkv[(long)tk * 1536 + 512 + t]; }
-  else if (tk <= -2) { int c = -2 - tk; q = qkv_pmt[c * 1536 + t]; k = qkv_pmt[c * 1536 + 512 + t]; }
-  long o = ((long)h * NG + g) * 64 + d;
-  Qg[o] = f2bf(q); Kg[o] = f2bf(k);
-}
-
-__global__ void k_gatherVt(const float* __restrict__ qkv, const float* __restrict__ qkv_pmt,
-                           const int* __restrict__ gtok, ushort* __restrict__ Vgt) {
-  int h = blockIdx.y, p0 = blockIdx.x * 64;
-  __shared__ float tile[64][65];
-  int tx = threadIdx.x & 63, tg = threadIdx.x >> 6;
-  for (int r = tg; r < 64; r += 4) {
-    int tk = gtok[p0 + r];
-    float v = 0.f;
-    if (tk >= 0)       v = qkv[(long)tk * 1536 + 1024 + h * 64 + tx];
-    else if (tk <= -2) v = qkv_pmt[(-2 - tk) * 1536 + 1024 + h * 64 + tx];
-    tile[r][tx] = v;
-  }
-  __syncthreads();
-  for (int d = tg; d < 64; d += 4) Vgt[((long)h * 64 + d) * NG + p0 + tx] = f2bf(tile[tx][d]);
+  for (int b = 0; b < 16; ++b) {
+    int n = b * 256 + t;
+    int c = idx[n];
+    sidx[t] = c;
+    __syncthreads();
+    int rank = 0;
+    for (int m = 0; m < t; ++m) rank += (sidx[m] == c);
+    int pos = boff[c][b] + rank;
+    gtok[pos] = n; gclu[pos] = c; gpos[n] = pos;
+    __syncthreads();
+  }
 }
 
 __global__ void k_outC(const float* __restrict__ OUTg, const int* __restrict__ gpos,
-                       const int* __restrict__ idx, const float* __restrict__ qkv,
-                       const float* __restrict__ qkv_pmt, const float* __restrict__ w,
-                       float* __restrict__ OUTA) {
+                       const int* __restrict__ idx, const float* __restrict__ qkvall,
+                       const float* __restrict__ w, ushort* __restrict__ lnb) {
   int n = blockIdx.x, t = threadIdx.x;
   int h = t >> 6;
   int c = idx[n];
@@ -542,11 +718,11 @@
   for (int tt = 0; tt < 33; ++tt) {
     int m = n + tt - 16;
     float vv = 0.f;
-    if (m == -1) vv = qkv_pmt[c * 1536 + 1024 + t];
-    else if (m >= 0 && m < NTOK && idx[m] == c) vv = qkv[(long)m * 1536 + 1024 + t];
+    if (m == -1) vv = qkvall[(long)c * 1536 + 1024 + t];
+    else if (m >= 0 && m < NTOK && idx[m] == c) vv = qkvall[(long)(8 + m) * 1536 + 1024 + t];
     acc += vv * w[h * 33 + tt];
   }
-  OUTA[(long)n * E + t] = acc;
+  lnb[(long)n * E + t] = f2bf(acc);
 }
 
 __global__ void k_seg_part(const float* __restrict__ hun, const int* __restrict__ idx,
@@ -594,17 +770,6 @@
     float e0 = expf(l0 - mx), e1 = expf(l1 - mx), s = e0 + e1;
     out[2] = e0 / s; out[3] = e1 / s;
     out[4] = *ptc;
-  }
-}
-
-static void pinv_iters(hipStream_t st, const ushort* PX, ushort* PZ, ushort* Y, ushort* T1, ushort* T2, int nb) {
-  ushort* z = PZ; ushort* y = Y;
-  for (int it = 0; it < 6; ++it) {
-    mm(st, PX, z,  nullptr, nullptr, nullptr, y,  256,256,256, nb,1,256, 65536,65536,65536, nullptr,nullptr,0,0,nullptr,0, 1.f,   0.f, 16,    false, false);
-    mm(st, y,  y,  nullptr, nullptr, nullptr, T1, 256,256,256, nb,1,256, 65536,65536,65536, nullptr,nullptr,0,0,nullptr,0, 1.f,   7.f, 16|4,  false, false);
-    mm(st, y,  T1, nullptr, nullptr, nullptr, T2, 256,256,256, nb,1,256, 65536,65536,65536, nullptr,nullptr,0,0,nullptr,0, 1.f,  15.f, 16|4,  false, false);
-    mm(st, z,  T2, nullptr, nullptr, nullptr, y,  256,256,256, nb,1,256, 65536,65536,65536, nullptr,nullptr,0,0,nullptr,0, 0.25f,13.f, 16|4,  false, false);
-    ushort* tmp = z; z = y; y = tmp;
   }
 }
 
@@ -641,14 +806,12 @@
   };
   float*  SEQ    = (float*) alloc((size_t)NSEQ * E * 4);
   float*  QKV    = (float*) alloc((size_t)NPAD * 1536 * 4);
-  float*  QKVPMT = (float*) alloc(8 * 1536 * 4);
   ushort* W1t    = (ushort*)alloc((size_t)512 * 1024 * 2);
   ushort* Wq1t   = (ushort*)alloc((size_t)1536 * 512 * 2);
   ushort* Wq0t   = (ushort*)alloc((size_t)1536 * 512 * 2);
   ushort* Wo1t   = (ushort*)alloc((size_t)512 * 512 * 2);
   ushort* Wo0t   = (ushort*)alloc((size_t)512 * 512 * 2);
   ushort* LNb    = (ushort*)alloc((size_t)NPAD * E * 2);
-  ushort* LNPMTb = (ushort*)alloc(8 * 512 * 2);
   ushort* QbU    = (ushort*)alloc((size_t)8 * NG * 64 * 2);
   ushort* KbU    = (ushort*)alloc((size_t)8 * NG * 64 * 2);
   ushort* VtU    = (ushort*)alloc((size_t)8 * NG * 64 * 2);
@@ -664,17 +827,12 @@
   ushort* avb    = (ushort*)alloc((size_t)64 * 16384 * 2);
   ushort* Wcb    = (ushort*)alloc((size_t)64 * 16384 * 2);
   float*  PREOUT = (float*) alloc((size_t)NPAD * E * 4);
-  float*  OUTA   = (float*) alloc((size_t)NTOK * E * 4);
-  float*  divB   = (float*) alloc(256 * 4);
   float*  mlandB = (float*) alloc(256 * 4);
-  float*  divC   = (float*) alloc(8 * 256 * 4);
   float*  mlandC = (float*) alloc(8 * 256 * 4);
   int*    idx    = (int*)   alloc(NTOK * 4);
   int*    gtok   = (int*)   alloc(NG * 4);
   int*    gclu   = (int*)   alloc(NG * 4);
   int*    gpos   = (int*)   alloc(NTOK * 4);
-  int*    scnt   = (int*)   alloc(8 * 16 * 4);
-  int*    boffA  = (int*)   alloc(8 * 16 * 4);
   int*    segb   = (int*)   alloc(9 * 4);
   int*    krange = (int*)   alloc(16 * 4);
   int*    blkclu = (int*)   alloc((NG / 128) * 4);
@@ -685,94 +843,71 @@
 
   ushort* hb   = (ushort*)U1;
   float*  Sbuf = (float*)U1;
-  ushort* Ybuf = (ushort*)U1;
-  ushort* T1   = (ushort*)(U1 + (size_t)64 * 65536 * 2);
-  ushort* T2   = (ushort*)(U1 + (size_t)2 * 64 * 65536 * 2);
+  ushort* ZBc  = (ushort*)U1;
+  ushort* T1c  = (ushort*)(U1 + (size_t)64 * 65536 * 2);
+  ushort* T2c  = (ushort*)(U1 + (size_t)2 * 64 * 65536 * 2);
   float*  OUTg = (float*)U1;
   ushort* Pbuf = (ushort*)U2;
 
-  k_tcvt<<<dim3(512/32, 1024/32), dim3(32,8), 0, stream>>>(W1, W1t, 1024, 512);
-  k_tcvt<<<dim3(1536/32, 512/32), dim3(32,8), 0, stream>>>(Wqkv1, Wq1t, 512, 1536);
-  k_tcvt<<<dim3(1536/32, 512/32), dim3(32,8), 0, stream>>>(Wqkv0, Wq0t, 512, 1536);
-  k_tcvt<<<dim3(512/32, 512/32),  dim3(32,8), 0, stream>>>(Wout1, Wo1t, 512, 512);
-  k_tcvt<<<dim3(512/32, 512/32),  dim3(32,8), 0, stream>>>(Wout0, Wo0t, 512, 512);
-
-  k_copy<<<dim3(2),  dim3(256), 0, stream>>>(cls,   SEQ,       512);
-  k_copy<<<dim3(16), dim3(256), 0, stream>>>(pmt_t, SEQ + 512, 4096);
+  k_tcvt_all<<<dim3(48, 32, 5), dim3(32, 8), 0, stream>>>(W1, Wqkv1, Wqkv0, Wout1, Wout0,
+                                                          W1t, Wq1t, Wq0t, Wo1t, Wo0t);
+  k_prep0<<<dim3(18), dim3(256), 0, stream>>>(cls, pmt_t, SEQ);
   k_cvt<<<dim3(16384), dim3(256), 0, stream>>>(h_in, hb, (long)4096 * 1024);
   mm(stream, hb, W1t, b1, nullptr, SEQ + 9 * 512, nullptr, 4096, 512, 1024, 1, 1, 512,
      0, 0, 0, nullptr, nullptr, 0, 0, nullptr, 0, 1.f, 0.f, 1 | 2, true, false);
 
-  hipMemsetAsync(LNb, 0, (size_t)PAD1 * E * 2, stream);
-  k_ln<<<dim3(NSEQ), dim3(256), 0, stream>>>(SEQ, ln1_g, ln1_b, LNb + (long)PAD1 * E, NSEQ);
+  k_lnB<<<dim3(NPAD), dim3(256), 0, stream>>>(SEQ, ln1_g, ln1_b, LNb);
   mm(stream, LNb, Wq1t, nullptr, nullptr, QKV, nullptr, NPAD, 1536, 512, 1, 1, 1536,
      0, 0, 0, nullptr, nullptr, 0, 0, nullptr, 0, 1.f, 0.f, 0, true, false);
-  k_buildK<<<dim3((NPAD*512)/256), dim3(256), 0, stream>>>(QKV, QbU, NPAD, 0);
-  k_buildK<<<dim3((NPAD*512)/256), dim3(256), 0, stream>>>(QKV, KbU, NPAD, 512);
-  k_buildVt<<<dim3(NPAD/64, 8), dim3(256), 0, stream>>>(QKV, VtU, NPAD);
-  k_lm_B<<<dim3(1), dim3(256), 0, stream>>>(divB, mlandB);
-  k_qlkl_B<<<dim3(256, 8), dim3(64), 0, stream>>>(QKV, divB, qlbB, klbB);
+  k_buildQKVB<<<dim3(NPAD / 64, 8), dim3(256), 0, stream>>>(QKV, QbU, KbU, VtU);
+  k_qlkl_B<<<dim3(256, 8), dim3(64), 0, stream>>>(QKV, qlbB, klbB, mlandB);
   mm(stream, qlbB, klbB, nullptr, nullptr, Sbuf, nullptr, 256, 256, 64, 8, 1, 256,
      16384, 16384, 65536, nullptr, nullptr, 0, 0, nullptr, 0, 1.f, 0.f, 0, true, false);
   k_a2soft<<<dim3(256, 8), dim3(256), 0, stream>>>(Sbuf, mlandB, PXb);
-  k_pinv_scale<<<dim3(1), dim3(256), 0, stream>>>(PXb, sc, 8);
-  k_z0<<<dim3((8*65536)/256), dim3(256), 0, stream>>>(PXb, sc, PZa, 8);
-  pinv_iters(stream, PXb, PZa, Ybuf, T1, T2, 8);
+  k_colmax<<<dim3(1), dim3(256), 0, stream>>>(PXb, sc);
+  k_pinv_chain<<<dim3(8), dim3(512), 0, stream>>>(PXb, PZa, ZBc, T1c, T2c, sc);
   mm(stream, qlbB, KbU, nullptr, nullptr, Sbuf, nullptr, 256, NPAD, 64, 8, 1, NPAD,
-     16384, (long)NPAD*64, (long)256*NPAD, nullptr, nullptr, 0, 0, nullptr, 0, 1.f, 0.f, 0, true, false);
+     16384, (long)NPAD * 64, (long)256 * NPAD, nullptr, nullptr, 0, 0, nullptr, 0, 1.f, 0.f, 0, true, false);
   k_smaxB_av<<<dim3(256, 8), dim3(256), 0, stream>>>(Sbuf, Pbuf, mlandB);
   mm(stream, Pbuf, VtU, nullptr, nullptr, avsl, nullptr, 256, 64, NPAD, 8, 8, 64,
-     (long)256*NPAD, (long)64*NPAD, 16384, nullptr, nullptr, 0, 0, nullptr, 0, 1.f, 0.f, 0, true, true);
+     (long)256 * NPAD, (long)64 * NPAD, 16384, nullptr, nullptr, 0, 0, nullptr, 0, 1.f, 0.f, 0, true, true);
   k_avredB<<<dim3(256, 8), dim3(64), 0, stream>>>(avsl, avb, 8);
   mm(stream, PZa, avb, nullptr, nullptr, nullptr, Wcb, 256, 64, 256, 8, 1, 64,
      65536, 16384, 16384, nullptr, nullptr, 0, 0, nullptr, 0, 1.f, 0.f, 16, false, true);
-  mm(stream, QbU + PAD1*64, klbB, nullptr, nullptr, Sbuf, nullptr, NSEQ, 256, 64, 8, 1, 256,
-     (long)NPAD*64, 16384, (long)NSEQ*256, nullptr, nullptr, 0, 0, nullptr, 0, 0.125f, 0.f, 0, true, true);
+  mm(stream, QbU + PAD1 * 64, klbB, nullptr, nullptr, Sbuf, nullptr, NSEQ, 256, 64, 8, 1, 256,
+     (long)NPAD * 64, 16384, (long)NSEQ * 256, nullptr, nullptr, 0, 0, nullptr, 0, 0.125f, 0.f, 0, true, true);
   k_smax256<0><<<dim3(NSEQ, 8), dim3(256), 0, stream>>>(Sbuf, Pbuf, mlandB, nullptr, nullptr, NSEQ);
-  mm(stream, Pbuf, Wcb, nullptr, nullptr, PREOUT + (long)PAD1*512, nullptr, NSEQ, 64, 256, 8, 1, 512,
-     (long)NSEQ*256, 16384, 64, nullptr, nullptr, 0, 0, nullptr, 0, 1.f, 0.f, 0, false, true);
-  k_conv_B<<<dim3(NSEQ), dim3(512), 0, stream>>>(QKV, conv1, PREOUT);
-  k_cvt<<<dim3((NSEQ*512 + 255)/256), dim3(256), 0, stream>>>(PREOUT + (long)PAD1*E, LNb, (long)NSEQ * 512);
+  mm(stream, Pbuf, Wcb, nullptr, nullptr, PREOUT + (long)PAD1 * 512, nullptr, NSEQ, 64, 256, 8, 1, 512,
+     (long)NSEQ * 256, 16384, 64, nullptr, nullptr, 0, 0, nullptr, 0, 1.f, 0.f, 0, false, true);
+  k_conv_B<<<dim3(NSEQ), dim3(512), 0, stream>>>(QKV, conv1, PREOUT, LNb);
   mm(stream, LNb, Wo1t, bout1, SEQ, SEQ, nullptr, NSEQ, 512, 512, 1, 1, 512,
      0, 0, 0, nullptr, nullptr, 0, 0, nullptr, 0, 1.f, 0.f, 1 | 8, true, true);
 
-  k_idx<<<dim3(NTOK), dim3(64), 0, stream>>>(SEQ, idx);
-  k_ptc<<<dim3(1), dim3(64), 0, stream>>>(SEQ, ptc);
-  hipMemsetAsync(gtok, 0xFF, NG * 4, stream);
-  hipMemsetAsync(gclu, 0xFF, NG * 4, stream);
-  k_gcnt<<<dim3(16), dim3(256), 0, stream>>>(idx, scnt);
-  k_goff<<<dim3(1), dim3(64), 0, stream>>>(scnt, segb, boffA, krange, blkclu, gtok, gclu);
-  k_gscatter<<<dim3(16), dim3(256), 0, stream>>>(idx, boffA, gtok, gclu, gpos);
-  k_ln<<<dim3(NTOK), dim3(256), 0, stream>>>(SEQ + 9 * 512, ln0_g, ln0_b, LNb, NTOK);
-  k_ln<<<dim3(8), dim3(256), 0, stream>>>(SEQ + 512, ln0_g, ln0_b, LNPMTb, 8);
-  mm(stream, LNb, Wq0t, nullptr, nullptr, QKV, nullptr, NTOK, 1536, 512, 1, 1, 1536,
-     0, 0, 0, nullptr, nullptr, 0, 0, nullptr, 0, 1.f, 0.f, 0, true, false);
-  mm(stream, LNPMTb, Wq0t, nullptr, nullptr, QKVPMT, nullptr, 8, 1536, 512, 1, 1, 1536,
+  k_idxptc<<<dim3(NTOK + 1), dim3(64), 0, stream>>>(SEQ, idx, ptc);
+  k_gprep<<<dim3(1), dim3(256), 0, stream>>>(idx, gtok, gclu, gpos, segb, krange, blkclu);
+  k_lnC<<<dim3(NTP), dim3(256), 0, stream>>>(SEQ, ln0_g, ln0_b, LNb);
+  mm(stream, LNb, Wq0t, nullptr, nullptr, QKV, nullptr, NTP, 1536, 512, 1, 1, 1536,
      0, 0, 0, nullptr, nullptr, 0, 0, nullptr, 0, 1.f, 0.f, 0, true, true);
-  k_lm_C<<<dim3(8), dim3(256), 0, stream>>>(idx, divC, mlandC);
-  k_qlkl_C<<<dim3(256, 64), dim3(64), 0, stream>>>(QKV, QKVPMT, idx, divC, qlcb, klcb);
-  k_gatherQK<<<dim3((NG*512)/256), dim3(256), 0, stream>>>(QKV, QKVPMT, gtok, QbU, KbU);
-  k_gatherVt<<<dim3(NG/64, 8), dim3(256), 0, stream>>>(QKV, QKVPMT, gtok, VtU);
+  k_qlkl_C<<<dim3(256, 64), dim3(64), 0, stream>>>(QKV, idx, qlcb, klcb, mlandC);
+  k_gatherQKV<<<dim3(NG / 64, 8), dim3(256), 0, stream>>>(QKV, gtok, QbU, KbU, VtU);
   mm(stream, qlcb, klcb, nullptr, nullptr, Sbuf, nullptr, 256, 256, 64, 64, 1, 256,
      16384, 16384, 65536, nullptr, nullptr, 0, 0, nullptr, 0, 1.f, 0.f, 0, true, false);
   k_a2soft<<<dim3(256, 64), dim3(256), 0, stream>>>(Sbuf, mlandC, PXb);
-  k_pinv_scale<<<dim3(8), dim3(256), 0, stream>>>(PXb, sc, 8);
-  k_z0<<<dim3((64*65536)/256), dim3(256), 0, stream>>>(PXb, sc, PZa, 64);
-  pinv_iters(stream, PXb, PZa, Ybuf, T1, T2, 64);
+  k_colmax<<<dim3(8), dim3(256), 0, stream>>>(PXb, sc);
+  k_pinv_chain<<<dim3(64), dim3(512), 0, stream>>>(PXb, PZa, ZBc, T1c, T2c, sc);
   mm(stream, qlcb, KbU, nullptr, nullptr, Sbuf, nullptr, 256, NG, 64, 8, 1, NG,
-     16384, (long)NG*64, (long)256*NG, blkclu, nullptr, 0, 0, nullptr, 0, 1.f, 0.f, 0, true, false);
+     16384, (long)NG * 64, (long)256 * NG, blkclu, nullptr, 0, 0, nullptr, 0, 1.f, 0.f, 0, true, false);
   k_smaxseg<<<dim3(256, 64), dim3(256), 0, stream>>>(Sbuf, Pbuf, mlandC, gclu, segb);
   mm(stream, Pbuf, VtU, nullptr, nullptr, nullptr, avb, 256, 64, NG, 64, 1, 64,
-     (long)256*NG, (long)64*NG, 16384, nullptr, nullptr, 8, 8, krange, 3, 1.f, 0.f, 16, true, true);
+     (long)256 * NG, (long)64 * NG, 16384, nullptr, nullptr, 8, 8, krange, 3, 1.f, 0.f, 16, true, true);
   mm(stream, PZa, avb, nullptr, nullptr, nullptr, Wcb, 256, 64, 256, 64, 1, 64,
      65536, 16384, 16384, nullptr, nullptr, 0, 0, nullptr, 0, 1.f, 0.f, 16, false, true);
   mm(stream, QbU, klcb, nullptr, nullptr, Sbuf, nullptr, NG, 256, 64, 8, 1, 256,
-     (long)NG*64, 16384, (long)NG*256, nullptr, blkclu, 0, 0, nullptr, 0, 0.125f, 0.f, 0, true, false);
+     (long)NG * 64, 16384, (long)NG * 256, nullptr, blkclu, 0, 0, nullptr, 0, 0.125f, 0.f, 0, true, false);
   k_smax256<1><<<dim3(NG, 8), dim3(256), 0, stream>>>(Sbuf, Pbuf, mlandC, gtok, gclu, NG);
   mm(stream, Pbuf, Wcb, nullptr, nullptr, OUTg, nullptr, NG, 64, 256, 8, 1, 512,
-     (long)NG*256, 16384, 64, nullptr, blkclu, 0, 0, nullptr, 0, 1.f, 0.f, 0, false, true);
-  k_outC<<<dim3(NTOK), dim3(512), 0, stream>>>(OUTg, gpos, idx, QKV, QKVPMT, conv0, OUTA);
-  k_cvt<<<dim3((NTOK*512)/256), dim3(256), 0, stream>>>(OUTA, LNb, (long)NTOK * 512);
+     (long)NG * 256, 16384, 64, nullptr, blkclu, 0, 0, nullptr, 0, 1.f, 0.f, 0, false, true);
+  k_outC<<<dim3(NTOK), dim3(512), 0, stream>>>(OUTg, gpos, idx, QKV, conv0, LNb);
   mm(stream, LNb, Wo0t, bout0, SEQ + 9 * 512, PREOUT, nullptr, NTOK, 512, 512, 1, 1, 512,
      0, 0, 0, nullptr, nullptr, 0, 0, nullptr, 0, 1.f, 0.f, 1 | 8, true, false);
 
```

New measurement: 2.513 ms. 7.3% less time.
